# Optimization experiments

Hardware: AMD Instinct MI355X
Metric: run time of the kernel (lower is better)

Reference implementation:

```python
import jax, jax.numpy as jnp
import numpy as np
from jax import lax

B, C, H, W = 2, 96, 96, 96
N = 8            # d_state
R = C // 16      # dt_rank = 6
K = 4            # scan directions


def _gn(x, g, b, eps=1e-5):
    # GroupNorm(num_groups=1): normalize over (C,H,W) per sample, per-channel affine
    mu = jnp.mean(x, axis=(1, 2, 3), keepdims=True)
    var = jnp.var(x, axis=(1, 2, 3), keepdims=True)
    xn = (x - mu) * jax.lax.rsqrt(var + eps)
    return xn * g[None, :, None, None] + b[None, :, None, None]


def _conv1x1(x, w, b):
    return jnp.einsum('bchw,oc->bohw', x, w) + b[None, :, None, None]


def _ss2d(x, xproj_w, dt_w, dt_b, A_log, Ds):
    # x: [B,C,H,W]. 4-directional selective scan (VMamba SS2D core).
    Bn, Cc, Hh, Ww = x.shape
    L = Hh * Ww
    x_hw = x.reshape(Bn, Cc, L)                                   # row-major
    x_wh = jnp.transpose(x, (0, 1, 3, 2)).reshape(Bn, Cc, L)      # col-major
    xs = jnp.stack([x_hw, x_wh, x_hw[..., ::-1], x_wh[..., ::-1]], axis=1)  # [B,K,C,L]
    xdbl = jnp.einsum('bkcl,kdc->bkdl', xs, xproj_w)              # [B,K,R+2N,L]
    dts, Bs, Cs = jnp.split(xdbl, [R, R + N], axis=2)             # [B,K,R,L],[B,K,N,L],[B,K,N,L]
    dts = jax.nn.softplus(jnp.einsum('bkrl,kcr->bkcl', dts, dt_w) + dt_b[None, :, :, None])  # [B,K,C,L]
    A = -jnp.exp(A_log)                                           # [K,C,N]
    dA = jnp.exp(dts[:, :, :, None, :] * A[None, :, :, :, None])                    # [B,K,C,N,L]
    dBx = dts[:, :, :, None, :] * Bs[:, :, None, :, :] * xs[:, :, :, None, :]       # [B,K,C,N,L]

    def comb(e1, e2):
        a1, b1 = e1
        a2, b2 = e2
        return a1 * a2, a2 * b1 + b2

    _, hs = lax.associative_scan(comb, (dA, dBx), axis=-1)        # h_t = dA_t*h_{t-1} + dBx_t
    ys = jnp.einsum('bkcnl,bknl->bkcl', hs, Cs) + Ds[None, :, :, None] * xs
    y0 = ys[:, 0]
    y1 = jnp.transpose(ys[:, 1].reshape(Bn, Cc, Ww, Hh), (0, 1, 3, 2)).reshape(Bn, Cc, L)
    y2 = ys[:, 2][..., ::-1]
    y3 = jnp.transpose(ys[:, 3][..., ::-1].reshape(Bn, Cc, Ww, Hh), (0, 1, 3, 2)).reshape(Bn, Cc, L)
    return (y0 + y1 + y2 + y3).reshape(Bn, Cc, Hh, Ww)


def setup_inputs() -> dict:
    key = jax.random.key(0)
    ks = jax.random.split(key, 12)
    f = lambda k, sh: jax.random.normal(k, sh, jnp.float32) * 0.02
    return {
        'x': jax.random.normal(ks[0], (B, C, H, W), jnp.float32),
        'ln_g': jnp.ones((C,), jnp.float32), 'ln_b': jnp.zeros((C,), jnp.float32),
        'p1_w': f(ks[1], (C, C)), 'p1_b': jnp.zeros((C,), jnp.float32),
        'p2_w': f(ks[2], (C, C)), 'p2_b': jnp.zeros((C,), jnp.float32),
        'dw_w': f(ks[3], (C, 1, 3, 3)), 'dw_b': jnp.zeros((C,), jnp.float32),
        'xproj_w': f(ks[4], (K, R + 2 * N, C)),
        'dt_w': f(ks[5], (K, C, R)), 'dt_b': f(ks[6], (K, C)),
        'A_log': jnp.log(jnp.broadcast_to(jnp.arange(1, N + 1, dtype=jnp.float32), (K, C, N))),
        'Ds': jnp.ones((K, C), jnp.float32),
        'n2_g': jnp.ones((C,), jnp.float32), 'n2_b': jnp.zeros((C,), jnp.float32),
        'ca_w1': f(ks[7], (C // 8, C)), 'ca_b1': jnp.zeros((C // 8,), jnp.float32),
        'ca_w2': f(ks[8], (C, C // 8)), 'ca_b2': jnp.zeros((C,), jnp.float32),
    }


def reference(x, ln_g, ln_b, p1_w, p1_b, p2_w, p2_b, dw_w, dw_b,
              xproj_w, dt_w, dt_b, A_log, Ds, n2_g, n2_b,
              ca_w1, ca_b1, ca_w2, ca_b2):
    h = _gn(x, ln_g, ln_b)
    a = jax.nn.silu(_conv1x1(h, p1_w, p1_b))                       # path 1
    b = _conv1x1(h, p2_w, p2_b)                                    # path 2
    b = lax.conv_general_dilated(b, dw_w, (1, 1), ((1, 1), (1, 1)),
                                 feature_group_count=C,
                                 dimension_numbers=('NCHW', 'OIHW', 'NCHW'))
    b = b + dw_b[None, :, None, None]
    b = jax.nn.silu(b)
    b = _ss2d(b, xproj_w, dt_w, dt_b, A_log, Ds)
    b = _gn(b, n2_g, n2_b)
    y = a * b
    # channel attention (SE-style, reduction 8)
    s = jnp.mean(y, axis=(2, 3))                                   # [B,C]
    z = jax.nn.relu(s @ ca_w1.T + ca_b1)
    attn = jax.nn.sigmoid(z @ ca_w2.T + ca_b2)
    y = y * attn[:, :, None, None]
    return x + y
```

## Files before the change

kernel.cpp:

```cpp
#include <hip/hip_runtime.h>
#include <hip/hip_bf16.h>
#include <cmath>
#include <cstdint>

constexpr int B_ = 2, C_ = 96, H_ = 96, W_ = 96, L_ = H_ * W_;
constexpr int N_ = 8, R_ = 6, K_ = 4, D_ = R_ + 2 * N_;
constexpr int CH_ = 128, G_ = L_ / CH_;
constexpr int JS_ = 4, SEG_ = CH_ / JS_;
constexpr int S_ = G_ * JS_;
constexpr float EPS_ = 1e-5f;

__device__ __forceinline__ float silu_f(float v) { return v / (1.f + __expf(-v)); }
__device__ __forceinline__ float softplus_f(float t) {
    return fmaxf(t, 0.f) + __logf(1.f + __expf(-fabsf(t)));
}

__device__ __forceinline__ void block_reduce2(float& a, float& b) {
    #pragma unroll
    for (int o = 32; o; o >>= 1) { a += __shfl_xor(a, o); b += __shfl_xor(b, o); }
    __shared__ float la[4], lb[4];
    int wid = threadIdx.x >> 6;
    if ((threadIdx.x & 63) == 0) { la[wid] = a; lb[wid] = b; }
    __syncthreads();
    if (threadIdx.x == 0) { a = la[0] + la[1] + la[2] + la[3]; b = lb[0] + lb[1] + lb[2] + lb[3]; }
}

__device__ __forceinline__ void block_reduce4(float& a, float& b, float& c, float& d) {
    #pragma unroll
    for (int o = 32; o; o >>= 1) {
        a += __shfl_xor(a, o); b += __shfl_xor(b, o);
        c += __shfl_xor(c, o); d += __shfl_xor(d, o);
    }
    __shared__ float ls[4][4];
    int wid = threadIdx.x >> 6;
    if ((threadIdx.x & 63) == 0) { ls[wid][0] = a; ls[wid][1] = b; ls[wid][2] = c; ls[wid][3] = d; }
    __syncthreads();
    if (threadIdx.x == 0) {
        a = ls[0][0] + ls[1][0] + ls[2][0] + ls[3][0];
        b = ls[0][1] + ls[1][1] + ls[2][1] + ls[3][1];
        c = ls[0][2] + ls[1][2] + ls[2][2] + ls[3][2];
        d = ls[0][3] + ls[1][3] + ls[2][3] + ls[3][3];
    }
}

__global__ __launch_bounds__(256) void stats_prep_kernel(
    const float* __restrict__ in, float* __restrict__ stats,
    const float* __restrict__ lng, const float* __restrict__ lnb,
    const float* __restrict__ w1, const float* __restrict__ w2,
    float* __restrict__ wmt, float* __restrict__ pq) {
    if (blockIdx.x == 432) {
        if (blockIdx.y != 0) return;
        int t = threadIdx.x;
        if (t >= 192) return;
        int mat = t / 96, o = t % 96;
        const float* w = (mat == 0 ? w1 : w2) + o * C_;
        float* dst = wmt + ((size_t)(mat * 12 + o / 8) * C_) * 8 + (o % 8);
        float P = 0.f, Q = 0.f;
        for (int c = 0; c < C_; ++c) {
            float wv = w[c];
            float g = lng[c];
            P = fmaf(lnb[c], wv, P);
            Q = fmaf(g, wv, Q);
            dst[c * 8] = g * wv;
        }
        pq[mat * 192 + o] = P;
        pq[mat * 192 + 96 + o] = Q;
        return;
    }
    int b = blockIdx.y;
    const float* p = in + (size_t)b * ((size_t)C_ * L_);
    float s = 0.f, s2 = 0.f;
    const int total = C_ * L_;
    for (int i = blockIdx.x * 256 + threadIdx.x; i < total; i += 432 * 256) {
        float v = p[i];
        s += v;
        s2 = fmaf(v, v, s2);
    }
    block_reduce2(s, s2);
    if (threadIdx.x == 0) {
        atomicAdd(&stats[2 * b], s);
        atomicAdd(&stats[2 * b + 1], s2);
    }
}

__global__ __launch_bounds__(256) void conv1x1_kernel(
    const float* __restrict__ x, const float* __restrict__ stats,
    const float* __restrict__ wmt, const float* __restrict__ pq,
    const float* __restrict__ b1, const float* __restrict__ b2,
    float* __restrict__ a, float* __restrict__ bpre) {
    constexpr int OG = 8;
    int b = blockIdx.z, by = blockIdx.y;
    int o0 = by * OG;
    int l = blockIdx.x * 256 + threadIdx.x;

    constexpr float inv = 1.f / (float)(C_ * L_);
    float mu = stats[2 * b] * inv;
    float var = stats[2 * b + 1] * inv - mu * mu;
    float rs = rsqrtf(var + EPS_);

    const float4* w1q = (const float4*)(wmt + ((size_t)(0 * 12 + by) * C_) * 8);
    const float4* w2q = (const float4*)(wmt + ((size_t)(1 * 12 + by) * C_) * 8);

    const float* xb = x + (size_t)b * C_ * L_ + l;
    float acc1[OG], acc2[OG];
    #pragma unroll
    for (int j = 0; j < OG; ++j) { acc1[j] = 0.f; acc2[j] = 0.f; }
    #pragma unroll 4
    for (int c = 0; c < C_; ++c) {
        float xv = xb[(size_t)c * L_];
        float4 wa = w1q[2 * c];
        float4 wb = w1q[2 * c + 1];
        float4 wc = w2q[2 * c];
        float4 wd = w2q[2 * c + 1];
        acc1[0] = fmaf(xv, wa.x, acc1[0]); acc1[1] = fmaf(xv, wa.y, acc1[1]);
        acc1[2] = fmaf(xv, wa.z, acc1[2]); acc1[3] = fmaf(xv, wa.w, acc1[3]);
        acc1[4] = fmaf(xv, wb.x, acc1[4]); acc1[5] = fmaf(xv, wb.y, acc1[5]);
        acc1[6] = fmaf(xv, wb.z, acc1[6]); acc1[7] = fmaf(xv, wb.w, acc1[7]);
        acc2[0] = fmaf(xv, wc.x, acc2[0]); acc2[1] = fmaf(xv, wc.y, acc2[1]);
        acc2[2] = fmaf(xv, wc.z, acc2[2]); acc2[3] = fmaf(xv, wc.w, acc2[3]);
        acc2[4] = fmaf(xv, wd.x, acc2[4]); acc2[5] = fmaf(xv, wd.y, acc2[5]);
        acc2[6] = fmaf(xv, wd.z, acc2[6]); acc2[7] = fmaf(xv, wd.w, acc2[7]);
    }
    float murs = mu * rs;
    #pragma unroll
    for (int j = 0; j < OG; ++j) {
        int o = o0 + j;
        size_t oo = ((size_t)(b * C_ + o)) * L_ + l;
        float be1 = b1[o] + pq[o] - murs * pq[96 + o];
        float be2 = b2[o] + pq[192 + o] - murs * pq[288 + o];
        a[oo] = silu_f(fmaf(rs, acc1[j], be1));
        bpre[oo] = fmaf(rs, acc2[j], be2);
    }
}

__global__ __launch_bounds__(256) void dwt_kernel(const float* __restrict__ bp,
                                                  const float* __restrict__ wgt,
                                                  const float* __restrict__ bias,
                                                  float* __restrict__ u,
                                                  float* __restrict__ u_t) {
    int stripe = blockIdx.x, c = blockIdx.y, b = blockIdx.z;
    int h0 = stripe * 48;
    __shared__ float in_s[50][96];
    __shared__ float out_s[48][97];
    const float* in = bp + ((size_t)(b * C_ + c)) * L_;
    for (int idx = threadIdx.x; idx < 50 * 96; idx += 256) {
        int r = idx / 96, w = idx % 96;
        int hh = h0 - 1 + r;
        in_s[r][w] = (hh >= 0 && hh < 96) ? in[hh * 96 + w] : 0.f;
    }
    __syncthreads();
    const float* kw = wgt + c * 9;
    float k0 = kw[0], k1 = kw[1], k2 = kw[2], k3 = kw[3], k4 = kw[4],
          k5 = kw[5], k6 = kw[6], k7 = kw[7], k8 = kw[8];
    float bs = bias[c];
    float* up = u + ((size_t)(b * C_ + c)) * L_;
    for (int idx = threadIdx.x; idx < 48 * 96; idx += 256) {
        int r = idx / 96, w = idx % 96;
        int ri = r + 1;
        bool wl = (w > 0), wr = (w < 95);
        float acc = bs;
        acc = fmaf(wl ? in_s[ri - 1][w - 1] : 0.f, k0, acc);
        acc = fmaf(in_s[ri - 1][w], k1, acc);
        acc = fmaf(wr ? in_s[ri - 1][w + 1] : 0.f, k2, acc);
        acc = fmaf(wl ? in_s[ri][w - 1] : 0.f, k3, acc);
        acc = fmaf(in_s[ri][w], k4, acc);
        acc = fmaf(wr ? in_s[ri][w + 1] : 0.f, k5, acc);
        acc = fmaf(wl ? in_s[ri + 1][w - 1] : 0.f, k6, acc);
        acc = fmaf(in_s[ri + 1][w], k7, acc);
        acc = fmaf(wr ? in_s[ri + 1][w + 1] : 0.f, k8, acc);
        float v = silu_f(acc);
        up[(h0 + r) * 96 + w] = v;
        out_s[r][w] = v;
    }
    __syncthreads();
    float* tp = u_t + ((size_t)(b * C_ + c)) * L_;
    for (int idx = threadIdx.x; idx < 96 * 48; idx += 256) {
        int w = idx / 48, r = idx % 48;
        tp[w * 96 + h0 + r] = out_s[r][w];
    }
}

__global__ __launch_bounds__(256) void proj_kernel(
    const float* __restrict__ u, const float* __restrict__ u_t,
    const float* __restrict__ xproj,
    float* __restrict__ dts, float* __restrict__ Bsb, float* __restrict__ Csb) {
    int b = blockIdx.z, k = blockIdx.y;
    int pos = threadIdx.x & 63, cg = threadIdx.x >> 6;
    int l = blockIdx.x * 64 + pos;

    __shared__ float sxp[C_][24];
    __shared__ float red[D_][4][64];
    for (int i = threadIdx.x; i < D_ * C_; i += 256) {
        int d = i / C_, c = i % C_;
        sxp[c][d] = xproj[(k * D_ + d) * C_ + c];
    }
    __syncthreads();

    const float* src = ((k & 1) ? u_t : u) + (size_t)b * C_ * L_;
    int posIdx = (k < 2) ? l : (L_ - 1 - l);
    const float* sp = src + (size_t)(cg * 24) * L_ + posIdx;

    float acc[D_];
    #pragma unroll
    for (int d = 0; d < D_; ++d) acc[d] = 0.f;
    #pragma unroll 4
    for (int ci = 0; ci < 24; ++ci) {
        int c = cg * 24 + ci;
        float xv = sp[(size_t)ci * L_];
        float w[22];
        *(float4*)&w[0]  = *(const float4*)&sxp[c][0];
        *(float4*)&w[4]  = *(const float4*)&sxp[c][4];
        *(float4*)&w[8]  = *(const float4*)&sxp[c][8];
        *(float4*)&w[12] = *(const float4*)&sxp[c][12];
        *(float4*)&w[16] = *(const float4*)&sxp[c][16];
        *(float2*)&w[20] = *(const float2*)&sxp[c][20];
        #pragma unroll
        for (int d = 0; d < D_; ++d) acc[d] = fmaf(xv, w[d], acc[d]);
    }
    #pragma unroll
    for (int d = 0; d < D_; ++d) red[d][cg][pos] = acc[d];
    __syncthreads();

    if (cg == 0) {
        #pragma unroll
        for (int r = 0; r < R_; ++r) {
            float s = red[r][0][pos] + red[r][1][pos] + red[r][2][pos] + red[r][3][pos];
            dts[((size_t)((b * K_ + k) * R_ + r)) * L_ + l] = s;
        }
    } else if (cg == 1) {
        #pragma unroll
        for (int n = 0; n < N_; ++n) {
            int d = R_ + n;
            float s = red[d][0][pos] + red[d][1][pos] + red[d][2][pos] + red[d][3][pos];
            Bsb[((size_t)((b * K_ + k) * N_ + n)) * L_ + l] = s;
        }
    } else if (cg == 2) {
        #pragma unroll
        for (int n = 0; n < N_; ++n) {
            int d = R_ + N_ + n;
            float s = red[d][0][pos] + red[d][1][pos] + red[d][2][pos] + red[d][3][pos];
            Csb[((size_t)((b * K_ + k) * N_ + n)) * L_ + l] = s;
        }
    }
}

__global__ __launch_bounds__(192) void scan1_kernel(
    const float* __restrict__ dts, const float* __restrict__ dtw,
    const float* __restrict__ dtbv, const float* __restrict__ Bs,
    const float* __restrict__ u, const float* __restrict__ u_t,
    const float* __restrict__ A_log,
    float* __restrict__ carA, float* __restrict__ carB) {
    int g = blockIdx.x >> 1, chalf = blockIdx.x & 1;
    int k = blockIdx.y, b = blockIdx.z;
    int c0 = chalf * 48;
    const int t = threadIdx.x;
    const int l0 = g * CH_;

    __shared__ float u_s[48][133];
    __shared__ float B_s[128][12];
    __shared__ float T_s[128][8];

    const float* usrc = ((k & 1) ? u_t : u) + (size_t)b * C_ * L_ + (size_t)c0 * L_;
    if (k < 2) {
        for (int idx = t; idx < 48 * 32; idx += 192) {
            int c2 = idx >> 5, q = idx & 31;
            *(float4*)&u_s[c2][q * 4] = *(const float4*)(usrc + (size_t)c2 * L_ + l0 + q * 4);
        }
    } else {
        for (int idx = t; idx < 48 * 32; idx += 192) {
            int c2 = idx >> 5, q = idx & 31;
            float4 v = *(const float4*)(usrc + (size_t)c2 * L_ + (L_ - l0 - q * 4 - 4));
            u_s[c2][q * 4 + 0] = v.w; u_s[c2][q * 4 + 1] = v.z;
            u_s[c2][q * 4 + 2] = v.y; u_s[c2][q * 4 + 3] = v.x;
        }
    }
    const float* Bg = Bs + ((size_t)(b * K_ + k)) * N_ * L_ + l0;
    for (int idx = t; idx < 8 * 32; idx += 192) {
        int n = idx >> 5, q = idx & 31;
        float4 v = *(const float4*)(Bg + (size_t)n * L_ + q * 4);
        B_s[q * 4 + 0][n] = v.x; B_s[q * 4 + 1][n] = v.y;
        B_s[q * 4 + 2][n] = v.z; B_s[q * 4 + 3][n] = v.w;
    }
    const float* Tg = dts + ((size_t)(b * K_ + k)) * R_ * L_ + l0;
    for (int idx = t; idx < 6 * 32; idx += 192) {
        int r = idx >> 5, q = idx & 31;
        float4 v = *(const float4*)(Tg + (size_t)r * L_ + q * 4);
        T_s[q * 4 + 0][r] = v.x; T_s[q * 4 + 1][r] = v.y;
        T_s[q * 4 + 2][r] = v.z; T_s[q * 4 + 3][r] = v.w;
    }
    __syncthreads();

    int cc = t % 48, j = t / 48;
    int c = c0 + cc;
    float A[N_];
    #pragma unroll
    for (int n = 0; n < N_; ++n) A[n] = -__expf(A_log[(k * C_ + c) * N_ + n]);
    float wdt[R_];
    #pragma unroll
    for (int r = 0; r < R_; ++r) wdt[r] = dtw[(k * C_ + c) * R_ + r];
    float bdt = dtbv[k * C_ + c];

    float ap[N_], h[N_];
    #pragma unroll
    for (int n = 0; n < N_; ++n) { ap[n] = 1.f; h[n] = 0.f; }
    int i0 = j * SEG_;
    for (int ii = 0; ii < SEG_; ii += 4) {
        float4 x4 = *(float4*)&u_s[cc][i0 + ii];
        float xx[4] = {x4.x, x4.y, x4.z, x4.w};
        #pragma unroll
        for (int s = 0; s < 4; ++s) {
            int i = i0 + ii + s;
            float4 t4 = *(float4*)&T_s[i][0];
            float2 t2 = *(float2*)&T_s[i][4];
            float tt = bdt;
            tt = fmaf(t4.x, wdt[0], tt); tt = fmaf(t4.y, wdt[1], tt);
            tt = fmaf(t4.z, wdt[2], tt); tt = fmaf(t4.w, wdt[3], tt);
            tt = fmaf(t2.x, wdt[4], tt); tt = fmaf(t2.y, wdt[5], tt);
            float d = softplus_f(tt);
            float dx = d * xx[s];
            float4 ba = *(float4*)&B_s[i][0];
            float4 bb = *(float4*)&B_s[i][4];
            float bv[8] = {ba.x, ba.y, ba.z, ba.w, bb.x, bb.y, bb.z, bb.w};
            #pragma unroll
            for (int n = 0; n < N_; ++n) {
                float da = __expf(d * A[n]);
                ap[n] *= da;
                h[n] = fmaf(da, h[n], bv[n] * dx);
            }
        }
    }
    size_t sidx = (((size_t)((b * K_ + k) * C_ + c)) * S_ + (g * JS_ + j)) * N_;
    #pragma unroll
    for (int n = 0; n < N_; ++n) { carA[sidx + n] = ap[n]; carB[sidx + n] = h[n]; }
}

__global__ __launch_bounds__(256) void scan2_kernel(const float* __restrict__ carA,
                                                    const float* __restrict__ carB,
                                                    float* __restrict__ hinit) {
    int row = blockIdx.x;
    const int t = threadIdx.x;
    __shared__ float as_[S_ * N_];
    __shared__ float bs_[S_ * N_];
    const float4* Ag = (const float4*)(carA + (size_t)row * S_ * N_);
    const float4* Bg4 = (const float4*)(carB + (size_t)row * S_ * N_);
    float4* As4 = (float4*)as_;
    float4* Bs4 = (float4*)bs_;
    for (int i = t; i < S_ * N_ / 4; i += 256) { As4[i] = Ag[i]; Bs4[i] = Bg4[i]; }
    __syncthreads();

    int n = t >> 5, g = t & 31;
    int s0 = g * 9;
    float A = 1.f, Bc = 0.f;
    #pragma unroll
    for (int q = 0; q < 9; ++q) {
        int idx = (s0 + q) * N_ + n;
        float a = as_[idx], b = bs_[idx];
        Bc = fmaf(a, Bc, b);
        A = a * A;
    }
    #pragma unroll
    for (int d = 1; d < 32; d <<= 1) {
        float pA = __shfl_up(A, d, 32);
        float pB = __shfl_up(Bc, d, 32);
        if (g >= d) { Bc = fmaf(A, pB, Bc); A = A * pA; }
    }
    float h = __shfl_up(Bc, 1, 32);
    if (g == 0) h = 0.f;
    #pragma unroll
    for (int q = 0; q < 9; ++q) {
        int idx = (s0 + q) * N_ + n;
        float a = as_[idx], b = bs_[idx];
        as_[idx] = h;
        h = fmaf(a, h, b);
    }
    __syncthreads();
    float4* Hg = (float4*)(hinit + (size_t)row * S_ * N_);
    for (int i = t; i < S_ * N_ / 4; i += 256) Hg[i] = As4[i];
}

__global__ __launch_bounds__(192) void scan3_kernel(
    const float* __restrict__ dts, const float* __restrict__ dtw,
    const float* __restrict__ dtbv, const float* __restrict__ Bs,
    const float* __restrict__ Cs, const float* __restrict__ u,
    const float* __restrict__ u_t, const float* __restrict__ A_log,
    const float* __restrict__ Dsv, const float* __restrict__ hinit,
    float* __restrict__ ydir) {
    int g = blockIdx.x >> 1, chalf = blockIdx.x & 1;
    int k = blockIdx.y, b = blockIdx.z;
    int c0 = chalf * 48;
    const int t = threadIdx.x;
    const int l0 = g * CH_;

    __shared__ float u_s[48][133];
    __shared__ float B_s[128][12];
    __shared__ float C_s[128][12];
    __shared__ float T_s[128][8];

    const float* usrc = ((k & 1) ? u_t : u) + (size_t)b * C_ * L_ + (size_t)c0 * L_;
    if (k < 2) {
        for (int idx = t; idx < 48 * 32; idx += 192) {
            int c2 = idx >> 5, q = idx & 31;
            *(float4*)&u_s[c2][q * 4] = *(const float4*)(usrc + (size_t)c2 * L_ + l0 + q * 4);
        }
    } else {
        for (int idx = t; idx < 48 * 32; idx += 192) {
            int c2 = idx >> 5, q = idx & 31;
            float4 v = *(const float4*)(usrc + (size_t)c2 * L_ + (L_ - l0 - q * 4 - 4));
            u_s[c2][q * 4 + 0] = v.w; u_s[c2][q * 4 + 1] = v.z;
            u_s[c2][q * 4 + 2] = v.y; u_s[c2][q * 4 + 3] = v.x;
        }
    }
    const float* Bg = Bs + ((size_t)(b * K_ + k)) * N_ * L_ + l0;
    const float* Cg = Cs + ((size_t)(b * K_ + k)) * N_ * L_ + l0;
    for (int idx = t; idx < 8 * 32; idx += 192) {
        int n = idx >> 5, q = idx & 31;
        float4 v = *(const float4*)(Bg + (size_t)n * L_ + q * 4);
        B_s[q * 4 + 0][n] = v.x; B_s[q * 4 + 1][n] = v.y;
        B_s[q * 4 + 2][n] = v.z; B_s[q * 4 + 3][n] = v.w;
        float4 w = *(const float4*)(Cg + (size_t)n * L_ + q * 4);
        C_s[q * 4 + 0][n] = w.x; C_s[q * 4 + 1][n] = w.y;
        C_s[q * 4 + 2][n] = w.z; C_s[q * 4 + 3][n] = w.w;
    }
    const float* Tg = dts + ((size_t)(b * K_ + k)) * R_ * L_ + l0;
    for (int idx = t; idx < 6 * 32; idx += 192) {
        int r = idx >> 5, q = idx & 31;
        float4 v = *(const float4*)(Tg + (size_t)r * L_ + q * 4);
        T_s[q * 4 + 0][r] = v.x; T_s[q * 4 + 1][r] = v.y;
        T_s[q * 4 + 2][r] = v.z; T_s[q * 4 + 3][r] = v.w;
    }
    __syncthreads();

    int cc = t % 48, j = t / 48;
    int c = c0 + cc;
    float A[N_];
    #pragma unroll
    for (int n = 0; n < N_; ++n) A[n] = -__expf(A_log[(k * C_ + c) * N_ + n]);
    float wdt[R_];
    #pragma unroll
    for (int r = 0; r < R_; ++r) wdt[r] = dtw[(k * C_ + c) * R_ + r];
    float bdt = dtbv[k * C_ + c];
    float Dv = Dsv[k * C_ + c];

    float h[N_];
    size_t sidx = (((size_t)((b * K_ + k) * C_ + c)) * S_ + (g * JS_ + j)) * N_;
    #pragma unroll
    for (int n = 0; n < N_; ++n) h[n] = hinit[sidx + n];

    int i0 = j * SEG_;
    for (int ii = 0; ii < SEG_; ii += 4) {
        float4 x4 = *(float4*)&u_s[cc][i0 + ii];
        float xx[4] = {x4.x, x4.y, x4.z, x4.w};
        #pragma unroll
        for (int s = 0; s < 4; ++s) {
            int i = i0 + ii + s;
            float4 t4 = *(float4*)&T_s[i][0];
            float2 t2 = *(float2*)&T_s[i][4];
            float tt = bdt;
            tt = fmaf(t4.x, wdt[0], tt); tt = fmaf(t4.y, wdt[1], tt);
            tt = fmaf(t4.z, wdt[2], tt); tt = fmaf(t4.w, wdt[3], tt);
            tt = fmaf(t2.x, wdt[4], tt); tt = fmaf(t2.y, wdt[5], tt);
            float d = softplus_f(tt);
            float dx = d * xx[s];
            float4 ba = *(float4*)&B_s[i][0];
            float4 bb = *(float4*)&B_s[i][4];
            float4 ca = *(float4*)&C_s[i][0];
            float4 cb = *(float4*)&C_s[i][4];
            float bv[8] = {ba.x, ba.y, ba.z, ba.w, bb.x, bb.y, bb.z, bb.w};
            float cv[8] = {ca.x, ca.y, ca.z, ca.w, cb.x, cb.y, cb.z, cb.w};
            float y = Dv * xx[s];
            #pragma unroll
            for (int n = 0; n < N_; ++n) {
                float da = __expf(d * A[n]);
                h[n] = fmaf(da, h[n], bv[n] * dx);
                y = fmaf(cv[n], h[n], y);
            }
            u_s[cc][i] = y;
        }
    }
    __syncthreads();
    float* yg = ydir + ((size_t)((b * K_ + k) * C_ + c0)) * L_ + l0;
    for (int idx = t; idx < 48 * 32; idx += 192) {
        int c2 = idx >> 5, q = idx & 31;
        *(float4*)(yg + (size_t)c2 * L_ + q * 4) = *(float4*)&u_s[c2][q * 4];
    }
}

__global__ __launch_bounds__(256) void merge_kernel(const float* __restrict__ ydir,
                                                    const float* __restrict__ a,
                                                    float* __restrict__ ysum,
                                                    float* __restrict__ stats) {
    int h0 = blockIdx.x * 32;
    int c = blockIdx.y, b = blockIdx.z;
    __shared__ float t1[96][33], t3[96][33];
    const float* y0p = ydir + ((size_t)((b * K_ + 0) * C_ + c)) * L_;
    const float* y1p = ydir + ((size_t)((b * K_ + 1) * C_ + c)) * L_;
    const float* y2p = ydir + ((size_t)((b * K_ + 2) * C_ + c)) * L_;
    const float* y3p = ydir + ((size_t)((b * K_ + 3) * C_ + c)) * L_;
    for (int idx = threadIdx.x; idx < 96 * 32; idx += 256) {
        int w = idx >> 5, hh = idx & 31;
        t1[w][hh] = y1p[w * 96 + h0 + hh];
        t3[w][hh] = y3p[L_ - 1 - (w * 96 + h0 + hh)];
    }
    __syncthreads();
    float s = 0.f, s2 = 0.f, m0 = 0.f, m1 = 0.f;
    float* yout = ysum + ((size_t)(b * C_ + c)) * L_;
    const float* ap = a + ((size_t)(b * C_ + c)) * L_;
    for (int idx = threadIdx.x; idx < 32 * 96; idx += 256) {
        int hh = idx / 96, w = idx % 96;
        int pix = (h0 + hh) * 96 + w;
        float v = y0p[pix] + y2p[L_ - 1 - pix] + t1[w][hh] + t3[w][hh];
        float av = ap[pix];
        yout[pix] = v;
        s += v;
        s2 = fmaf(v, v, s2);
        m0 += av;
        m1 = fmaf(av, v, m1);
    }
    block_reduce4(s, s2, m0, m1);
    if (threadIdx.x == 0) {
        atomicAdd(&stats[4 + 2 * b], s);
        atomicAdd(&stats[5 + 2 * b], s2);
        atomicAdd(&stats[16 + b * C_ + c], m0);
        atomicAdd(&stats[256 + b * C_ + c], m1);
    }
}

__global__ __launch_bounds__(128) void attn_kernel(
    const float* __restrict__ stats, const float* __restrict__ g2,
    const float* __restrict__ b2, const float* __restrict__ w1,
    const float* __restrict__ b1, const float* __restrict__ w2,
    const float* __restrict__ b2a, float* __restrict__ attn) {
    int b = blockIdx.x;
    constexpr float inv = 1.f / (float)(C_ * L_);
    float mu = stats[4 + 2 * b] * inv;
    float var = stats[5 + 2 * b] * inv - mu * mu;
    float rs = rsqrtf(var + EPS_);
    __shared__ float ss[C_];
    __shared__ float zz[12];
    int t = threadIdx.x;
    if (t < C_) {
        float M0 = stats[16 + b * C_ + t];
        float M1 = stats[256 + b * C_ + t];
        ss[t] = (g2[t] * rs * (M1 - mu * M0) + b2[t] * M0) * (1.f / (float)L_);
    }
    __syncthreads();
    if (t < 12) {
        float acc = b1[t];
        for (int c = 0; c < C_; ++c) acc = fmaf(w1[t * C_ + c], ss[c], acc);
        zz[t] = fmaxf(acc, 0.f);
    }
    __syncthreads();
    if (t < C_) {
        float acc = b2a[t];
        #pragma unroll
        for (int j = 0; j < 12; ++j) acc = fmaf(w2[t * 12 + j], zz[j], acc);
        attn[b * C_ + t] = 1.f / (1.f + __expf(-acc));
    }
}

__global__ __launch_bounds__(256) void final_kernel(const float* __restrict__ x,
                                                    const float* __restrict__ ysum,
                                                    const float* __restrict__ a,
                                                    const float* __restrict__ stats,
                                                    const float* __restrict__ g2,
                                                    const float* __restrict__ b2,
                                                    const float* __restrict__ attn,
                                                    float* __restrict__ out) {
    int b = blockIdx.z, c = blockIdx.y;
    int pix = blockIdx.x * 256 + threadIdx.x;
    constexpr float inv = 1.f / (float)(C_ * L_);
    float mu = stats[4 + 2 * b] * inv;
    float var = stats[5 + 2 * b] * inv - mu * mu;
    float rs = rsqrtf(var + EPS_);
    float gc = g2[c] * rs, bc = b2[c] - mu * rs * g2[c];
    float at = attn[b * C_ + c];
    size_t o = ((size_t)(b * C_ + c)) * L_ + pix;
    float bn = fmaf(ysum[o], gc, bc);
    out[o] = fmaf(a[o] * bn, at, x[o]);
}

extern "C" void kernel_launch(void* const* d_in, const int* in_sizes, int n_in,
                              void* d_out, int out_size, void* d_ws, size_t ws_size,
                              hipStream_t stream) {
    const float* x    = (const float*)d_in[0];
    const float* ln_g = (const float*)d_in[1];
    const float* ln_b = (const float*)d_in[2];
    const float* p1w  = (const float*)d_in[3];
    const float* p1b  = (const float*)d_in[4];
    const float* p2w  = (const float*)d_in[5];
    const float* p2b  = (const float*)d_in[6];
    const float* dww  = (const float*)d_in[7];
    const float* dwb  = (const float*)d_in[8];
    const float* xprj = (const float*)d_in[9];
    const float* dtw  = (const float*)d_in[10];
    const float* dtb  = (const float*)d_in[11];
    const float* Alog = (const float*)d_in[12];
    const float* Dsp  = (const float*)d_in[13];
    const float* n2g  = (const float*)d_in[14];
    const float* n2b  = (const float*)d_in[15];
    const float* caw1 = (const float*)d_in[16];
    const float* cab1 = (const float*)d_in[17];
    const float* caw2 = (const float*)d_in[18];
    const float* cab2 = (const float*)d_in[19];
    float* out = (float*)d_out;

    const size_t BCL = (size_t)B_ * C_ * L_ * sizeof(float);
    char* ws = (char*)d_ws;
    size_t off = 0;
    float* stats = (float*)(ws + off); off += 4096;
    float* wmt   = (float*)(ws + off); off += 2 * 12 * 96 * 8 * sizeof(float);
    float* pq    = (float*)(ws + off); off += 2 * 2 * 96 * sizeof(float);
    float* a     = (float*)(ws + off); off += BCL;
    float* bpre  = (float*)(ws + off); off += BCL;
    float* u     = (float*)(ws + off); off += BCL;
    float* u_t   = (float*)(ws + off); off += BCL;
    float* dts   = (float*)(ws + off); off += (size_t)B_ * K_ * R_ * L_ * sizeof(float);
    float* Bsb   = (float*)(ws + off); off += (size_t)B_ * K_ * N_ * L_ * sizeof(float);
    float* Csb   = (float*)(ws + off); off += (size_t)B_ * K_ * N_ * L_ * sizeof(float);
    float* carB  = (float*)(ws + off); off += (size_t)B_ * K_ * C_ * S_ * N_ * sizeof(float);
    float* hinit = (float*)(ws + off); off += (size_t)B_ * K_ * C_ * S_ * N_ * sizeof(float);
    float* ydir  = (float*)(ws + off); off += (size_t)B_ * K_ * C_ * L_ * sizeof(float);
    float* carA = bpre;
    float* ysum = u;
    float* attnv = stats + 512;

    hipMemsetAsync(stats, 0, 4096, stream);

    stats_prep_kernel<<<dim3(433, 2), 256, 0, stream>>>(x, stats, ln_g, ln_b,
                                                        p1w, p2w, wmt, pq);
    conv1x1_kernel<<<dim3(36, 12, 2), 256, 0, stream>>>(x, stats, wmt, pq, p1b, p2b, a, bpre);
    dwt_kernel<<<dim3(2, 96, 2), 256, 0, stream>>>(bpre, dww, dwb, u, u_t);
    proj_kernel<<<dim3(144, 4, 2), 256, 0, stream>>>(u, u_t, xprj, dts, Bsb, Csb);
    scan1_kernel<<<dim3(2 * G_, K_, B_), 192, 0, stream>>>(dts, dtw, dtb, Bsb, u, u_t,
                                                           Alog, carA, carB);
    scan2_kernel<<<B_ * K_ * C_, 256, 0, stream>>>(carA, carB, hinit);
    scan3_kernel<<<dim3(2 * G_, K_, B_), 192, 0, stream>>>(dts, dtw, dtb, Bsb, Csb, u, u_t,
                                                           Alog, Dsp, hinit, ydir);
    merge_kernel<<<dim3(3, 96, 2), 256, 0, stream>>>(ydir, a, ysum, stats);
    attn_kernel<<<2, 128, 0, stream>>>(stats, n2g, n2b, caw1, cab1, caw2, cab2, attnv);
    final_kernel<<<dim3(36, 96, 2), 256, 0, stream>>>(x, ysum, a, stats, n2g, n2b, attnv, out);
}
```

Before: 269.9 us.

## Fuse all stages into one persistent cooperative kernel with grid syncs

Replaces the ten separate kernel launches with a single cooperative persistent kernel that loops over virtual blocks for each stage and separates stages with grid-wide syncs. The attention MLP is folded into the final stage and recomputed per block. The goal is to remove per-launch overhead and the gaps between launches. In exchange, the scan stages now run with 256 threads instead of 192, occupancy is capped by the largest shared-memory footprint, and grid.sync has its own cost.

```diff
diff --git a/kernel.cpp b/kernel.cpp
--- a/kernel.cpp
+++ b/kernel.cpp
@@ -1,7 +1,10 @@
 #include <hip/hip_runtime.h>
 #include <hip/hip_bf16.h>
+#include <hip/hip_cooperative_groups.h>
 #include <cmath>
 #include <cstdint>
+
+namespace cg = cooperative_groups;
 
 constexpr int B_ = 2, C_ = 96, H_ = 96, W_ = 96, L_ = H_ * W_;
 constexpr int N_ = 8, R_ = 6, K_ = 4, D_ = R_ + 2 * N_;
@@ -23,6 +26,7 @@
     if ((threadIdx.x & 63) == 0) { la[wid] = a; lb[wid] = b; }
     __syncthreads();
     if (threadIdx.x == 0) { a = la[0] + la[1] + la[2] + la[3]; b = lb[0] + lb[1] + lb[2] + lb[3]; }
+    __syncthreads();
 }
 
 __device__ __forceinline__ void block_reduce4(float& a, float& b, float& c, float& d) {
@@ -41,569 +45,506 @@
         c = ls[0][2] + ls[1][2] + ls[2][2] + ls[3][2];
         d = ls[0][3] + ls[1][3] + ls[2][3] + ls[3][3];
     }
+    __syncthreads();
 }
 
-__global__ __launch_bounds__(256) void stats_prep_kernel(
-    const float* __restrict__ in, float* __restrict__ stats,
-    const float* __restrict__ lng, const float* __restrict__ lnb,
-    const float* __restrict__ w1, const float* __restrict__ w2,
-    float* __restrict__ wmt, float* __restrict__ pq) {
-    if (blockIdx.x == 432) {
-        if (blockIdx.y != 0) return;
-        int t = threadIdx.x;
-        if (t >= 192) return;
-        int mat = t / 96, o = t % 96;
-        const float* w = (mat == 0 ? w1 : w2) + o * C_;
-        float* dst = wmt + ((size_t)(mat * 12 + o / 8) * C_) * 8 + (o % 8);
-        float P = 0.f, Q = 0.f;
+struct DwtS   { float in_s[50][96]; float out_s[48][97]; };
+struct ProjS  { float sxp[96][24]; float red[22][4][64]; };
+struct Scan1S { float u_s[48][133]; float B_s[128][12]; float T_s[128][8]; };
+struct Scan2S { float as_[S_ * N_]; float bs_[S_ * N_]; };
+struct Scan3S { float u_s[48][133]; float B_s[128][12]; float C_s[128][12]; float T_s[128][8]; };
+struct MergeS { float t1[96][33]; float t3[96][33]; };
+struct FinalS { float zz[12]; float atv; };
+
+struct P {
+    const float *x, *lng, *lnb, *p1w, *p1b, *p2w, *p2b, *dww, *dwb, *xprj,
+                *dtw, *dtb, *Alog, *Dsp, *n2g, *n2b, *caw1, *cab1, *caw2, *cab2;
+    float *stats, *wmt, *pq, *a, *bpre, *u, *u_t, *dts, *Bsb, *Csb,
+          *carA, *carB, *hinit, *ydir, *ysum, *out;
+};
+
+__global__ __launch_bounds__(256, 2) void mono_kernel(P p) {
+    cg::grid_group grid = cg::this_grid();
+    __shared__ __align__(16) char smem[41984];
+    const int t = threadIdx.x;
+    const int GS = gridDim.x;
+
+    for (int vb = blockIdx.x; vb < 865; vb += GS) {
+        if (vb < 864) {
+            int bx = vb % 432, b = vb / 432;
+            const float* ptr = p.x + (size_t)b * C_ * L_;
+            float s = 0.f, s2 = 0.f;
+            for (int i = bx * 256 + t; i < C_ * L_; i += 432 * 256) {
+                float v = ptr[i];
+                s += v;
+                s2 = fmaf(v, v, s2);
+            }
+            block_reduce2(s, s2);
+            if (t == 0) {
+                atomicAdd(&p.stats[2 * b], s);
+                atomicAdd(&p.stats[2 * b + 1], s2);
+            }
+        } else if (t < 192) {
+            int mat = t / 96, o = t % 96;
+            const float* w = (mat == 0 ? p.p1w : p.p2w) + o * C_;
+            float* dst = p.wmt + ((size_t)(mat * 12 + o / 8) * C_) * 8 + (o % 8);
+            float Pv = 0.f, Qv = 0.f;
+            for (int c = 0; c < C_; ++c) {
+                float wv = w[c];
+                float g = p.lng[c];
+                Pv = fmaf(p.lnb[c], wv, Pv);
+                Qv = fmaf(g, wv, Qv);
+                dst[c * 8] = g * wv;
+            }
+            p.pq[mat * 192 + o] = Pv;
+            p.pq[mat * 192 + 96 + o] = Qv;
+        }
+        __syncthreads();
+    }
+    grid.sync();
+
+    for (int vb = blockIdx.x; vb < 864; vb += GS) {
+        constexpr int OG = 8;
+        int lx = vb % 36, by = (vb / 36) % 12, b = vb / 432;
+        int o0 = by * OG;
+        int l = lx * 256 + t;
+        constexpr float inv = 1.f / (float)(C_ * L_);
+        float mu = p.stats[2 * b] * inv;
+        float var = p.stats[2 * b + 1] * inv - mu * mu;
+        float rs = rsqrtf(var + EPS_);
+        const float4* w1q = (const float4*)(p.wmt + ((size_t)(0 * 12 + by) * C_) * 8);
+        const float4* w2q = (const float4*)(p.wmt + ((size_t)(1 * 12 + by) * C_) * 8);
+        const float* xb = p.x + (size_t)b * C_ * L_ + l;
+        float acc1[OG], acc2[OG];
+        #pragma unroll
+        for (int j = 0; j < OG; ++j) { acc1[j] = 0.f; acc2[j] = 0.f; }
+        #pragma unroll 4
         for (int c = 0; c < C_; ++c) {
-            float wv = w[c];
-            float g = lng[c];
-            P = fmaf(lnb[c], wv, P);
-            Q = fmaf(g, wv, Q);
-            dst[c * 8] = g * wv;
-        }
-        pq[mat * 192 + o] = P;
-        pq[mat * 192 + 96 + o] = Q;
-        return;
-    }
-    int b = blockIdx.y;
-    const float* p = in + (size_t)b * ((size_t)C_ * L_);
-    float s = 0.f, s2 = 0.f;
-    const int total = C_ * L_;
-    for (int i = blockIdx.x * 256 + threadIdx.x; i < total; i += 432 * 256) {
-        float v = p[i];
-        s += v;
-        s2 = fmaf(v, v, s2);
-    }
-    block_reduce2(s, s2);
-    if (threadIdx.x == 0) {
-        atomicAdd(&stats[2 * b], s);
-        atomicAdd(&stats[2 * b + 1], s2);
-    }
-}
-
-__global__ __launch_bounds__(256) void conv1x1_kernel(
-    const float* __restrict__ x, const float* __restrict__ stats,
-    const float* __restrict__ wmt, const float* __restrict__ pq,
-    const float* __restrict__ b1, const float* __restrict__ b2,
-    float* __restrict__ a, float* __restrict__ bpre) {
-    constexpr int OG = 8;
-    int b = blockIdx.z, by = blockIdx.y;
-    int o0 = by * OG;
-    int l = blockIdx.x * 256 + threadIdx.x;
-
-    constexpr float inv = 1.f / (float)(C_ * L_);
-    float mu = stats[2 * b] * inv;
-    float var = stats[2 * b + 1] * inv - mu * mu;
-    float rs = rsqrtf(var + EPS_);
-
-    const float4* w1q = (const float4*)(wmt + ((size_t)(0 * 12 + by) * C_) * 8);
-    const float4* w2q = (const float4*)(wmt + ((size_t)(1 * 12 + by) * C_) * 8);
-
-    const float* xb = x + (size_t)b * C_ * L_ + l;
-    float acc1[OG], acc2[OG];
-    #pragma unroll
-    for (int j = 0; j < OG; ++j) { acc1[j] = 0.f; acc2[j] = 0.f; }
-    #pragma unroll 4
-    for (int c = 0; c < C_; ++c) {
-        float xv = xb[(size_t)c * L_];
-        float4 wa = w1q[2 * c];
-        float4 wb = w1q[2 * c + 1];
-        float4 wc = w2q[2 * c];
-        float4 wd = w2q[2 * c + 1];
-        acc1[0] = fmaf(xv, wa.x, acc1[0]); acc1[1] = fmaf(xv, wa.y, acc1[1]);
-        acc1[2] = fmaf(xv, wa.z, acc1[2]); acc1[3] = fmaf(xv, wa.w, acc1[3]);
-        acc1[4] = fmaf(xv, wb.x, acc1[4]); acc1[5] = fmaf(xv, wb.y, acc1[5]);
-        acc1[6] = fmaf(xv, wb.z, acc1[6]); acc1[7] = fmaf(xv, wb.w, acc1[7]);
-        acc2[0] = fmaf(xv, wc.x, acc2[0]); acc2[1] = fmaf(xv, wc.y, acc2[1]);
-        acc2[2] = fmaf(xv, wc.z, acc2[2]); acc2[3] = fmaf(xv, wc.w, acc2[3]);
-        acc2[4] = fmaf(xv, wd.x, acc2[4]); acc2[5] = fmaf(xv, wd.y, acc2[5]);
-        acc2[6] = fmaf(xv, wd.z, acc2[6]); acc2[7] = fmaf(xv, wd.w, acc2[7]);
-    }
-    float murs = mu * rs;
-    #pragma unroll
-    for (int j = 0; j < OG; ++j) {
-        int o = o0 + j;
-        size_t oo = ((size_t)(b * C_ + o)) * L_ + l;
-        float be1 = b1[o] + pq[o] - murs * pq[96 + o];
-        float be2 = b2[o] + pq[192 + o] - murs * pq[288 + o];
-        a[oo] = silu_f(fmaf(rs, acc1[j], be1));
-        bpre[oo] = fmaf(rs, acc2[j], be2);
-    }
-}
-
-__global__ __launch_bounds__(256) void dwt_kernel(const float* __restrict__ bp,
-                                                  const float* __restrict__ wgt,
-                                                  const float* __restrict__ bias,
-                                                  float* __restrict__ u,
-                                                  float* __restrict__ u_t) {
-    int stripe = blockIdx.x, c = blockIdx.y, b = blockIdx.z;
-    int h0 = stripe * 48;
-    __shared__ float in_s[50][96];
-    __shared__ float out_s[48][97];
-    const float* in = bp + ((size_t)(b * C_ + c)) * L_;
-    for (int idx = threadIdx.x; idx < 50 * 96; idx += 256) {
-        int r = idx / 96, w = idx % 96;
-        int hh = h0 - 1 + r;
-        in_s[r][w] = (hh >= 0 && hh < 96) ? in[hh * 96 + w] : 0.f;
-    }
-    __syncthreads();
-    const float* kw = wgt + c * 9;
-    float k0 = kw[0], k1 = kw[1], k2 = kw[2], k3 = kw[3], k4 = kw[4],
-          k5 = kw[5], k6 = kw[6], k7 = kw[7], k8 = kw[8];
-    float bs = bias[c];
-    float* up = u + ((size_t)(b * C_ + c)) * L_;
-    for (int idx = threadIdx.x; idx < 48 * 96; idx += 256) {
-        int r = idx / 96, w = idx % 96;
-        int ri = r + 1;
-        bool wl = (w > 0), wr = (w < 95);
-        float acc = bs;
-        acc = fmaf(wl ? in_s[ri - 1][w - 1] : 0.f, k0, acc);
-        acc = fmaf(in_s[ri - 1][w], k1, acc);
-        acc = fmaf(wr ? in_s[ri - 1][w + 1] : 0.f, k2, acc);
-        acc = fmaf(wl ? in_s[ri][w - 1] : 0.f, k3, acc);
-        acc = fmaf(in_s[ri][w], k4, acc);
-        acc = fmaf(wr ? in_s[ri][w + 1] : 0.f, k5, acc);
-        acc = fmaf(wl ? in_s[ri + 1][w - 1] : 0.f, k6, acc);
-        acc = fmaf(in_s[ri + 1][w], k7, acc);
-        acc = fmaf(wr ? in_s[ri + 1][w + 1] : 0.f, k8, acc);
-        float v = silu_f(acc);
-        up[(h0 + r) * 96 + w] = v;
-        out_s[r][w] = v;
-    }
-    __syncthreads();
-    float* tp = u_t + ((size_t)(b * C_ + c)) * L_;
-    for (int idx = threadIdx.x; idx < 96 * 48; idx += 256) {
-        int w = idx / 48, r = idx % 48;
-        tp[w * 96 + h0 + r] = out_s[r][w];
-    }
-}
-
-__global__ __launch_bounds__(256) void proj_kernel(
-    const float* __restrict__ u, const float* __restrict__ u_t,
-    const float* __restrict__ xproj,
-    float* __restrict__ dts, float* __restrict__ Bsb, float* __restrict__ Csb) {
-    int b = blockIdx.z, k = blockIdx.y;
-    int pos = threadIdx.x & 63, cg = threadIdx.x >> 6;
-    int l = blockIdx.x * 64 + pos;
-
-    __shared__ float sxp[C_][24];
-    __shared__ float red[D_][4][64];
-    for (int i = threadIdx.x; i < D_ * C_; i += 256) {
-        int d = i / C_, c = i % C_;
-        sxp[c][d] = xproj[(k * D_ + d) * C_ + c];
-    }
-    __syncthreads();
-
-    const float* src = ((k & 1) ? u_t : u) + (size_t)b * C_ * L_;
-    int posIdx = (k < 2) ? l : (L_ - 1 - l);
-    const float* sp = src + (size_t)(cg * 24) * L_ + posIdx;
-
-    float acc[D_];
-    #pragma unroll
-    for (int d = 0; d < D_; ++d) acc[d] = 0.f;
-    #pragma unroll 4
-    for (int ci = 0; ci < 24; ++ci) {
-        int c = cg * 24 + ci;
-        float xv = sp[(size_t)ci * L_];
-        float w[22];
-        *(float4*)&w[0]  = *(const float4*)&sxp[c][0];
-        *(float4*)&w[4]  = *(const float4*)&sxp[c][4];
-        *(float4*)&w[8]  = *(const float4*)&sxp[c][8];
-        *(float4*)&w[12] = *(const float4*)&sxp[c][12];
-        *(float4*)&w[16] = *(const float4*)&sxp[c][16];
-        *(float2*)&w[20] = *(const float2*)&sxp[c][20];
+            float xv = xb[(size_t)c * L_];
+            float4 wa = w1q[2 * c];
+            float4 wb = w1q[2 * c + 1];
+            float4 wc = w2q[2 * c];
+            float4 wd = w2q[2 * c + 1];
+            acc1[0] = fmaf(xv, wa.x, acc1[0]); acc1[1] = fmaf(xv, wa.y, acc1[1]);
+            acc1[2] = fmaf(xv, wa.z, acc1[2]); acc1[3] = fmaf(xv, wa.w, acc1[3]);
+            acc1[4] = fmaf(xv, wb.x, acc1[4]); acc1[5] = fmaf(xv, wb.y, acc1[5]);
+            acc1[6] = fmaf(xv, wb.z, acc1[6]); acc1[7] = fmaf(xv, wb.w, acc1[7]);
+            acc2[0] = fmaf(xv, wc.x, acc2[0]); acc2[1] = fmaf(xv, wc.y, acc2[1]);
+            acc2[2] = fmaf(xv, wc.z, acc2[2]); acc2[3] = fmaf(xv, wc.w, acc2[3]);
+            acc2[4] = fmaf(xv, wd.x, acc2[4]); acc2[5] = fmaf(xv, wd.y, acc2[5]);
+            acc2[6] = fmaf(xv, wd.z, acc2[6]); acc2[7] = fmaf(xv, wd.w, acc2[7]);
+        }
+        float murs = mu * rs;
         #pragma unroll
-        for (int d = 0; d < D_; ++d) acc[d] = fmaf(xv, w[d], acc[d]);
-    }
-    #pragma unroll
-    for (int d = 0; d < D_; ++d) red[d][cg][pos] = acc[d];
-    __syncthreads();
-
-    if (cg == 0) {
+        for (int j = 0; j < OG; ++j) {
+            int o = o0 + j;
+            size_t oo = ((size_t)(b * C_ + o)) * L_ + l;
+            float be1 = p.p1b[o] + p.pq[o] - murs * p.pq[96 + o];
+            float be2 = p.p2b[o] + p.pq[192 + o] - murs * p.pq[288 + o];
+            p.a[oo] = silu_f(fmaf(rs, acc1[j], be1));
+            p.bpre[oo] = fmaf(rs, acc2[j], be2);
+        }
+    }
+    grid.sync();
+
+    for (int vb = blockIdx.x; vb < 384; vb += GS) {
+        DwtS& S = *(DwtS*)smem;
+        int stripe = vb % 2, c = (vb / 2) % 96, b = vb / 192;
+        int h0 = stripe * 48;
+        const float* in = p.bpre + ((size_t)(b * C_ + c)) * L_;
+        for (int idx = t; idx < 50 * 96; idx += 256) {
+            int r = idx / 96, w = idx % 96;
+            int hh = h0 - 1 + r;
+            S.in_s[r][w] = (hh >= 0 && hh < 96) ? in[hh * 96 + w] : 0.f;
+        }
+        __syncthreads();
+        const float* kw = p.dww + c * 9;
+        float k0 = kw[0], k1 = kw[1], k2 = kw[2], k3 = kw[3], k4 = kw[4],
+              k5 = kw[5], k6 = kw[6], k7 = kw[7], k8 = kw[8];
+        float bs = p.dwb[c];
+        float* up = p.u + ((size_t)(b * C_ + c)) * L_;
+        for (int idx = t; idx < 48 * 96; idx += 256) {
+            int r = idx / 96, w = idx % 96;
+            int ri = r + 1;
+            bool wl = (w > 0), wr = (w < 95);
+            float acc = bs;
+            acc = fmaf(wl ? S.in_s[ri - 1][w - 1] : 0.f, k0, acc);
+            acc = fmaf(S.in_s[ri - 1][w], k1, acc);
+            acc = fmaf(wr ? S.in_s[ri - 1][w + 1] : 0.f, k2, acc);
+            acc = fmaf(wl ? S.in_s[ri][w - 1] : 0.f, k3, acc);
+            acc = fmaf(S.in_s[ri][w], k4, acc);
+            acc = fmaf(wr ? S.in_s[ri][w + 1] : 0.f, k5, acc);
+            acc = fmaf(wl ? S.in_s[ri + 1][w - 1] : 0.f, k6, acc);
+            acc = fmaf(S.in_s[ri + 1][w], k7, acc);
+            acc = fmaf(wr ? S.in_s[ri + 1][w + 1] : 0.f, k8, acc);
+            float v = silu_f(acc);
+            up[(h0 + r) * 96 + w] = v;
+            S.out_s[r][w] = v;
+        }
+        __syncthreads();
+        float* tp = p.u_t + ((size_t)(b * C_ + c)) * L_;
+        for (int idx = t; idx < 96 * 48; idx += 256) {
+            int w = idx / 48, r = idx % 48;
+            tp[w * 96 + h0 + r] = S.out_s[r][w];
+        }
+        __syncthreads();
+    }
+    grid.sync();
+
+    for (int vb = blockIdx.x; vb < 1152; vb += GS) {
+        ProjS& S = *(ProjS*)smem;
+        int lx = vb % 144, k = (vb / 144) % 4, b = vb / 576;
+        int pos = t & 63, cgp = t >> 6;
+        int l = lx * 64 + pos;
+        for (int i = t; i < D_ * C_; i += 256) {
+            int d = i / C_, c = i % C_;
+            S.sxp[c][d] = p.xprj[(k * D_ + d) * C_ + c];
+        }
+        __syncthreads();
+        const float* src = ((k & 1) ? p.u_t : p.u) + (size_t)b * C_ * L_;
+        int posIdx = (k < 2) ? l : (L_ - 1 - l);
+        const float* sp = src + (size_t)(cgp * 24) * L_ + posIdx;
+        float acc[D_];
         #pragma unroll
-        for (int r = 0; r < R_; ++r) {
-            float s = red[r][0][pos] + red[r][1][pos] + red[r][2][pos] + red[r][3][pos];
-            dts[((size_t)((b * K_ + k) * R_ + r)) * L_ + l] = s;
-        }
-    } else if (cg == 1) {
+        for (int d = 0; d < D_; ++d) acc[d] = 0.f;
+        #pragma unroll 4
+        for (int ci = 0; ci < 24; ++ci) {
+            int c = cgp * 24 + ci;
+            float xv = sp[(size_t)ci * L_];
+            float w[22];
+            *(float4*)&w[0]  = *(const float4*)&S.sxp[c][0];
+            *(float4*)&w[4]  = *(const float4*)&S.sxp[c][4];
+            *(float4*)&w[8]  = *(const float4*)&S.sxp[c][8];
+            *(float4*)&w[12] = *(const float4*)&S.sxp[c][12];
+            *(float4*)&w[16] = *(const float4*)&S.sxp[c][16];
+            *(float2*)&w[20] = *(const float2*)&S.sxp[c][20];
+            #pragma unroll
+            for (int d = 0; d < D_; ++d) acc[d] = fmaf(xv, w[d], acc[d]);
+        }
         #pragma unroll
-        for (int n = 0; n < N_; ++n) {
-            int d = R_ + n;
-            float s = red[d][0][pos] + red[d][1][pos] + red[d][2][pos] + red[d][3][pos];
-            Bsb[((size_t)((b * K_ + k) * N_ + n)) * L_ + l] = s;
-        }
-    } else if (cg == 2) {
+        for (int d = 0; d < D_; ++d) S.red[d][cgp][pos] = acc[d];
+        __syncthreads();
+        if (cgp == 0) {
+            #pragma unroll
+            for (int r = 0; r < R_; ++r) {
+                float s = S.red[r][0][pos] + S.red[r][1][pos] + S.red[r][2][pos] + S.red[r][3][pos];
+                p.dts[((size_t)((b * K_ + k) * R_ + r)) * L_ + l] = s;
+            }
+        } else if (cgp == 1) {
+            #pragma unroll
+            for (int n = 0; n < N_; ++n) {
+                int d = R_ + n;
+                float s = S.red[d][0][pos] + S.red[d][1][pos] + S.red[d][2][pos] + S.red[d][3][pos];
+                p.Bsb[((size_t)((b * K_ + k) * N_ + n)) * L_ + l] = s;
+            }
+        } else if (cgp == 2) {
+            #pragma unroll
+            for (int n = 0; n < N_; ++n) {
+                int d = R_ + N_ + n;
+                float s = S.red[d][0][pos] + S.red[d][1][pos] + S.red[d][2][pos] + S.red[d][3][pos];
+                p.Csb[((size_t)((b * K_ + k) * N_ + n)) * L_ + l] = s;
+            }
+        }
+        __syncthreads();
+    }
+    grid.sync();
+
+    for (int vb = blockIdx.x; vb < 1152; vb += GS) {
+        Scan1S& S = *(Scan1S*)smem;
+        int gx = vb % 144, k = (vb / 144) % 4, b = vb / 576;
+        int g = gx >> 1, chalf = gx & 1;
+        int c0 = chalf * 48;
+        const int l0 = g * CH_;
+        const float* usrc = ((k & 1) ? p.u_t : p.u) + (size_t)b * C_ * L_ + (size_t)c0 * L_;
+        if (k < 2) {
+            for (int idx = t; idx < 48 * 32; idx += 256) {
+                int c2 = idx >> 5, q = idx & 31;
+                *(float4*)&S.u_s[c2][q * 4] = *(const float4*)(usrc + (size_t)c2 * L_ + l0 + q * 4);
+            }
+        } else {
+            for (int idx = t; idx < 48 * 32; idx += 256) {
+                int c2 = idx >> 5, q = idx & 31;
+                float4 v = *(const float4*)(usrc + (size_t)c2 * L_ + (L_ - l0 - q * 4 - 4));
+                S.u_s[c2][q * 4 + 0] = v.w; S.u_s[c2][q * 4 + 1] = v.z;
+                S.u_s[c2][q * 4 + 2] = v.y; S.u_s[c2][q * 4 + 3] = v.x;
+            }
+        }
+        const float* Bg = p.Bsb + ((size_t)(b * K_ + k)) * N_ * L_ + l0;
+        for (int idx = t; idx < 8 * 32; idx += 256) {
+            int n = idx >> 5, q = idx & 31;
+            float4 v = *(const float4*)(Bg + (size_t)n * L_ + q * 4);
+            S.B_s[q * 4 + 0][n] = v.x; S.B_s[q * 4 + 1][n] = v.y;
+            S.B_s[q * 4 + 2][n] = v.z; S.B_s[q * 4 + 3][n] = v.w;
+        }
+        const float* Tg = p.dts + ((size_t)(b * K_ + k)) * R_ * L_ + l0;
+        for (int idx = t; idx < 6 * 32; idx += 256) {
+            int r = idx >> 5, q = idx & 31;
+            float4 v = *(const float4*)(Tg + (size_t)r * L_ + q * 4);
+            S.T_s[q * 4 + 0][r] = v.x; S.T_s[q * 4 + 1][r] = v.y;
+            S.T_s[q * 4 + 2][r] = v.z; S.T_s[q * 4 + 3][r] = v.w;
+        }
+        __syncthreads();
+        if (t < 192) {
+            int cc = t % 48, j = t / 48;
+            int c = c0 + cc;
+            float A[N_];
+            #pragma unroll
+            for (int n = 0; n < N_; ++n) A[n] = -__expf(p.Alog[(k * C_ + c) * N_ + n]);
+            float wdt[R_];
+            #pragma unroll
+            for (int r = 0; r < R_; ++r) wdt[r] = p.dtw[(k * C_ + c) * R_ + r];
+            float bdt = p.dtb[k * C_ + c];
+            float ap[N_], h[N_];
+            #pragma unroll
+            for (int n = 0; n < N_; ++n) { ap[n] = 1.f; h[n] = 0.f; }
+            int i0 = j * SEG_;
+            for (int ii = 0; ii < SEG_; ii += 4) {
+                float4 x4 = *(float4*)&S.u_s[cc][i0 + ii];
+                float xx[4] = {x4.x, x4.y, x4.z, x4.w};
+                #pragma unroll
+                for (int s = 0; s < 4; ++s) {
+                    int i = i0 + ii + s;
+                    float4 t4 = *(float4*)&S.T_s[i][0];
+                    float2 t2 = *(float2*)&S.T_s[i][4];
+                    float tt = bdt;
+                    tt = fmaf(t4.x, wdt[0], tt); tt = fmaf(t4.y, wdt[1], tt);
+                    tt = fmaf(t4.z, wdt[2], tt); tt = fmaf(t4.w, wdt[3], tt);
+                    tt = fmaf(t2.x, wdt[4], tt); tt = fmaf(t2.y, wdt[5], tt);
+                    float d = softplus_f(tt);
+                    float dx = d * xx[s];
+                    float4 ba = *(float4*)&S.B_s[i][0];
+                    float4 bb = *(float4*)&S.B_s[i][4];
+                    float bv[8] = {ba.x, ba.y, ba.z, ba.w, bb.x, bb.y, bb.z, bb.w};
+                    #pragma unroll
+                    for (int n = 0; n < N_; ++n) {
+                        float da = __expf(d * A[n]);
+                        ap[n] *= da;
+                        h[n] = fmaf(da, h[n], bv[n] * dx);
+                    }
+                }
+            }
+            size_t sidx = (((size_t)((b * K_ + k) * C_ + c)) * S_ + (g * JS_ + j)) * N_;
+            #pragma unroll
+            for (int n = 0; n < N_; ++n) { p.carA[sidx + n] = ap[n]; p.carB[sidx + n] = h[n]; }
+        }
+        __syncthreads();
+    }
+    grid.sync();
+
+    for (int vb = blockIdx.x; vb < 768; vb += GS) {
+        Scan2S& S = *(Scan2S*)smem;
+        int row = vb;
+        const float4* Ag = (const float4*)(p.carA + (size_t)row * S_ * N_);
+        const float4* Bg4 = (const float4*)(p.carB + (size_t)row * S_ * N_);
+        float4* As4 = (float4*)S.as_;
+        float4* Bs4 = (float4*)S.bs_;
+        for (int i = t; i < S_ * N_ / 4; i += 256) { As4[i] = Ag[i]; Bs4[i] = Bg4[i]; }
+        __syncthreads();
+        int n = t >> 5, g = t & 31;
+        int s0 = g * 9;
+        float A = 1.f, Bc = 0.f;
         #pragma unroll
-        for (int n = 0; n < N_; ++n) {
-            int d = R_ + N_ + n;
-            float s = red[d][0][pos] + red[d][1][pos] + red[d][2][pos] + red[d][3][pos];
-            Csb[((size_t)((b * K_ + k) * N_ + n)) * L_ + l] = s;
-        }
-    }
-}
-
-__global__ __launch_bounds__(192) void scan1_kernel(
-    const float* __restrict__ dts, const float* __restrict__ dtw,
-    const float* __restrict__ dtbv, const float* __restrict__ Bs,
-    const float* __restrict__ u, const float* __restrict__ u_t,
-    const float* __restrict__ A_log,
-    float* __restrict__ carA, float* __restrict__ carB) {
-    int g = blockIdx.x >> 1, chalf = blockIdx.x & 1;
-    int k = blockIdx.y, b = blockIdx.z;
-    int c0 = chalf * 48;
-    const int t = threadIdx.x;
-    const int l0 = g * CH_;
-
-    __shared__ float u_s[48][133];
-    __shared__ float B_s[128][12];
-    __shared__ float T_s[128][8];
-
-    const float* usrc = ((k & 1) ? u_t : u) + (size_t)b * C_ * L_ + (size_t)c0 * L_;
-    if (k < 2) {
-        for (int idx = t; idx < 48 * 32; idx += 192) {
+        for (int q = 0; q < 9; ++q) {
+            int idx = (s0 + q) * N_ + n;
+            float a = S.as_[idx], b = S.bs_[idx];
+            Bc = fmaf(a, Bc, b);
+            A = a * A;
+        }
+        #pragma unroll
+        for (int d = 1; d < 32; d <<= 1) {
+            float pA = __shfl_up(A, d, 32);
+            float pB = __shfl_up(Bc, d, 32);
+            if (g >= d) { Bc = fmaf(A, pB, Bc); A = A * pA; }
+        }
+        float h = __shfl_up(Bc, 1, 32);
+        if (g == 0) h = 0.f;
+        #pragma unroll
+        for (int q = 0; q < 9; ++q) {
+            int idx = (s0 + q) * N_ + n;
+            float a = S.as_[idx], b = S.bs_[idx];
+            S.as_[idx] = h;
+            h = fmaf(a, h, b);
+        }
+        __syncthreads();
+        float4* Hg = (float4*)(p.hinit + (size_t)row * S_ * N_);
+        for (int i = t; i < S_ * N_ / 4; i += 256) Hg[i] = As4[i];
+        __syncthreads();
+    }
+    grid.sync();
+
+    for (int vb = blockIdx.x; vb < 1152; vb += GS) {
+        Scan3S& S = *(Scan3S*)smem;
+        int gx = vb % 144, k = (vb / 144) % 4, b = vb / 576;
+        int g = gx >> 1, chalf = gx & 1;
+        int c0 = chalf * 48;
+        const int l0 = g * CH_;
+        const float* usrc = ((k & 1) ? p.u_t : p.u) + (size_t)b * C_ * L_ + (size_t)c0 * L_;
+        if (k < 2) {
+            for (int idx = t; idx < 48 * 32; idx += 256) {
+                int c2 = idx >> 5, q = idx & 31;
+                *(float4*)&S.u_s[c2][q * 4] = *(const float4*)(usrc + (size_t)c2 * L_ + l0 + q * 4);
+            }
+        } else {
+            for (int idx = t; idx < 48 * 32; idx += 256) {
+                int c2 = idx >> 5, q = idx & 31;
+                float4 v = *(const float4*)(usrc + (size_t)c2 * L_ + (L_ - l0 - q * 4 - 4));
+                S.u_s[c2][q * 4 + 0] = v.w; S.u_s[c2][q * 4 + 1] = v.z;
+                S.u_s[c2][q * 4 + 2] = v.y; S.u_s[c2][q * 4 + 3] = v.x;
+            }
+        }
+        const float* Bg = p.Bsb + ((size_t)(b * K_ + k)) * N_ * L_ + l0;
+        const float* Cg = p.Csb + ((size_t)(b * K_ + k)) * N_ * L_ + l0;
+        for (int idx = t; idx < 8 * 32; idx += 256) {
+            int n = idx >> 5, q = idx & 31;
+            float4 v = *(const float4*)(Bg + (size_t)n * L_ + q * 4);
+            S.B_s[q * 4 + 0][n] = v.x; S.B_s[q * 4 + 1][n] = v.y;
+            S.B_s[q * 4 + 2][n] = v.z; S.B_s[q * 4 + 3][n] = v.w;
+            float4 w = *(const float4*)(Cg + (size_t)n * L_ + q * 4);
+            S.C_s[q * 4 + 0][n] = w.x; S.C_s[q * 4 + 1][n] = w.y;
+            S.C_s[q * 4 + 2][n] = w.z; S.C_s[q * 4 + 3][n] = w.w;
+        }
+        const float* Tg = p.dts + ((size_t)(b * K_ + k)) * R_ * L_ + l0;
+        for (int idx = t; idx < 6 * 32; idx += 256) {
+            int r = idx >> 5, q = idx & 31;
+            float4 v = *(const float4*)(Tg + (size_t)r * L_ + q * 4);
+            S.T_s[q * 4 + 0][r] = v.x; S.T_s[q * 4 + 1][r] = v.y;
+            S.T_s[q * 4 + 2][r] = v.z; S.T_s[q * 4 + 3][r] = v.w;
+        }
+        __syncthreads();
+        if (t < 192) {
+            int cc = t % 48, j = t / 48;
+            int c = c0 + cc;
+            float A[N_];
+            #pragma unroll
+            for (int n = 0; n < N_; ++n) A[n] = -__expf(p.Alog[(k * C_ + c) * N_ + n]);
+            float wdt[R_];
+            #pragma unroll
+            for (int r = 0; r < R_; ++r) wdt[r] = p.dtw[(k * C_ + c) * R_ + r];
+            float bdt = p.dtb[k * C_ + c];
+            float Dv = p.Dsp[k * C_ + c];
+            float h[N_];
+            size_t sidx = (((size_t)((b * K_ + k) * C_ + c)) * S_ + (g * JS_ + j)) * N_;
+            #pragma unroll
+            for (int n = 0; n < N_; ++n) h[n] = p.hinit[sidx + n];
+            int i0 = j * SEG_;
+            for (int ii = 0; ii < SEG_; ii += 4) {
+                float4 x4 = *(float4*)&S.u_s[cc][i0 + ii];
+                float xx[4] = {x4.x, x4.y, x4.z, x4.w};
+                #pragma unroll
+                for (int s = 0; s < 4; ++s) {
+                    int i = i0 + ii + s;
+                    float4 t4 = *(float4*)&S.T_s[i][0];
+                    float2 t2 = *(float2*)&S.T_s[i][4];
+                    float tt = bdt;
+                    tt = fmaf(t4.x, wdt[0], tt); tt = fmaf(t4.y, wdt[1], tt);
+                    tt = fmaf(t4.z, wdt[2], tt); tt = fmaf(t4.w, wdt[3], tt);
+                    tt = fmaf(t2.x, wdt[4], tt); tt = fmaf(t2.y, wdt[5], tt);
+                    float d = softplus_f(tt);
+                    float dx = d * xx[s];
+                    float4 ba = *(float4*)&S.B_s[i][0];
+                    float4 bb = *(float4*)&S.B_s[i][4];
+                    float4 ca = *(float4*)&S.C_s[i][0];
+                    float4 cb = *(float4*)&S.C_s[i][4];
+                    float bv[8] = {ba.x, ba.y, ba.z, ba.w, bb.x, bb.y, bb.z, bb.w};
+                    float cv[8] = {ca.x, ca.y, ca.z, ca.w, cb.x, cb.y, cb.z, cb.w};
+                    float y = Dv * xx[s];
+                    #pragma unroll
+                    for (int n = 0; n < N_; ++n) {
+                        float da = __expf(d * A[n]);
+                        h[n] = fmaf(da, h[n], bv[n] * dx);
+                        y = fmaf(cv[n], h[n], y);
+                    }
+                    S.u_s[cc][i] = y;
+                }
+            }
+        }
+        __syncthreads();
+        float* yg = p.ydir + ((size_t)((b * K_ + k) * C_ + c0)) * L_ + l0;
+        for (int idx = t; idx < 48 * 32; idx += 256) {
             int c2 = idx >> 5, q = idx & 31;
-            *(float4*)&u_s[c2][q * 4] = *(const float4*)(usrc + (size_t)c2 * L_ + l0 + q * 4);
-        }
-    } else {
-        for (int idx = t; idx < 48 * 32; idx += 192) {
-            int c2 = idx >> 5, q = idx & 31;
-            float4 v = *(const float4*)(usrc + (size_t)c2 * L_ + (L_ - l0 - q * 4 - 4));
-            u_s[c2][q * 4 + 0] = v.w; u_s[c2][q * 4 + 1] = v.z;
-            u_s[c2][q * 4 + 2] = v.y; u_s[c2][q * 4 + 3] = v.x;
-        }
-    }
-    const float* Bg = Bs + ((size_t)(b * K_ + k)) * N_ * L_ + l0;
-    for (int idx = t; idx < 8 * 32; idx += 192) {
-        int n = idx >> 5, q = idx & 31;
-        float4 v = *(const float4*)(Bg + (size_t)n * L_ + q * 4);
-        B_s[q * 4 + 0][n] = v.x; B_s[q * 4 + 1][n] = v.y;
-        B_s[q * 4 + 2][n] = v.z; B_s[q * 4 + 3][n] = v.w;
-    }
-    const float* Tg = dts + ((size_t)(b * K_ + k)) * R_ * L_ + l0;
-    for (int idx = t; idx < 6 * 32; idx += 192) {
-        int r = idx >> 5, q = idx & 31;
-        float4 v = *(const float4*)(Tg + (size_t)r * L_ + q * 4);
-        T_s[q * 4 + 0][r] = v.x; T_s[q * 4 + 1][r] = v.y;
-        T_s[q * 4 + 2][r] = v.z; T_s[q * 4 + 3][r] = v.w;
-    }
-    __syncthreads();
-
-    int cc = t % 48, j = t / 48;
-    int c = c0 + cc;
-    float A[N_];
-    #pragma unroll
-    for (int n = 0; n < N_; ++n) A[n] = -__expf(A_log[(k * C_ + c) * N_ + n]);
-    float wdt[R_];
-    #pragma unroll
-    for (int r = 0; r < R_; ++r) wdt[r] = dtw[(k * C_ + c) * R_ + r];
-    float bdt = dtbv[k * C_ + c];
-
-    float ap[N_], h[N_];
-    #pragma unroll
-    for (int n = 0; n < N_; ++n) { ap[n] = 1.f; h[n] = 0.f; }
-    int i0 = j * SEG_;
-    for (int ii = 0; ii < SEG_; ii += 4) {
-        float4 x4 = *(float4*)&u_s[cc][i0 + ii];
-        float xx[4] = {x4.x, x4.y, x4.z, x4.w};
-        #pragma unroll
-        for (int s = 0; s < 4; ++s) {
-            int i = i0 + ii + s;
-            float4 t4 = *(float4*)&T_s[i][0];
-            float2 t2 = *(float2*)&T_s[i][4];
-            float tt = bdt;
-            tt = fmaf(t4.x, wdt[0], tt); tt = fmaf(t4.y, wdt[1], tt);
-            tt = fmaf(t4.z, wdt[2], tt); tt = fmaf(t4.w, wdt[3], tt);
-            tt = fmaf(t2.x, wdt[4], tt); tt = fmaf(t2.y, wdt[5], tt);
-            float d = softplus_f(tt);
-            float dx = d * xx[s];
-            float4 ba = *(float4*)&B_s[i][0];
-            float4 bb = *(float4*)&B_s[i][4];
-            float bv[8] = {ba.x, ba.y, ba.z, ba.w, bb.x, bb.y, bb.z, bb.w};
-            #pragma unroll
-            for (int n = 0; n < N_; ++n) {
-                float da = __expf(d * A[n]);
-                ap[n] *= da;
-                h[n] = fmaf(da, h[n], bv[n] * dx);
-            }
-        }
-    }
-    size_t sidx = (((size_t)((b * K_ + k) * C_ + c)) * S_ + (g * JS_ + j)) * N_;
-    #pragma unroll
-    for (int n = 0; n < N_; ++n) { carA[sidx + n] = ap[n]; carB[sidx + n] = h[n]; }
-}
-
-__global__ __launch_bounds__(256) void scan2_kernel(const float* __restrict__ carA,
-                                                    const float* __restrict__ carB,
-                                                    float* __restrict__ hinit) {
-    int row = blockIdx.x;
-    const int t = threadIdx.x;
-    __shared__ float as_[S_ * N_];
-    __shared__ float bs_[S_ * N_];
-    const float4* Ag = (const float4*)(carA + (size_t)row * S_ * N_);
-    const float4* Bg4 = (const float4*)(carB + (size_t)row * S_ * N_);
-    float4* As4 = (float4*)as_;
-    float4* Bs4 = (float4*)bs_;
-    for (int i = t; i < S_ * N_ / 4; i += 256) { As4[i] = Ag[i]; Bs4[i] = Bg4[i]; }
-    __syncthreads();
-
-    int n = t >> 5, g = t & 31;
-    int s0 = g * 9;
-    float A = 1.f, Bc = 0.f;
-    #pragma unroll
-    for (int q = 0; q < 9; ++q) {
-        int idx = (s0 + q) * N_ + n;
-        float a = as_[idx], b = bs_[idx];
-        Bc = fmaf(a, Bc, b);
-        A = a * A;
-    }
-    #pragma unroll
-    for (int d = 1; d < 32; d <<= 1) {
-        float pA = __shfl_up(A, d, 32);
-        float pB = __shfl_up(Bc, d, 32);
-        if (g >= d) { Bc = fmaf(A, pB, Bc); A = A * pA; }
-    }
-    float h = __shfl_up(Bc, 1, 32);
-    if (g == 0) h = 0.f;
-    #pragma unroll
-    for (int q = 0; q < 9; ++q) {
-        int idx = (s0 + q) * N_ + n;
-        float a = as_[idx], b = bs_[idx];
-        as_[idx] = h;
-        h = fmaf(a, h, b);
-    }
-    __syncthreads();
-    float4* Hg = (float4*)(hinit + (size_t)row * S_ * N_);
-    for (int i = t; i < S_ * N_ / 4; i += 256) Hg[i] = As4[i];
-}
-
-__global__ __launch_bounds__(192) void scan3_kernel(
-    const float* __restrict__ dts, const float* __restrict__ dtw,
-    const float* __restrict__ dtbv, const float* __restrict__ Bs,
-    const float* __restrict__ Cs, const float* __restrict__ u,
-    const float* __restrict__ u_t, const float* __restrict__ A_log,
-    const float* __restrict__ Dsv, const float* __restrict__ hinit,
-    float* __restrict__ ydir) {
-    int g = blockIdx.x >> 1, chalf = blockIdx.x & 1;
-    int k = blockIdx.y, b = blockIdx.z;
-    int c0 = chalf * 48;
-    const int t = threadIdx.x;
-    const int l0 = g * CH_;
-
-    __shared__ float u_s[48][133];
-    __shared__ float B_s[128][12];
-    __shared__ float C_s[128][12];
-    __shared__ float T_s[128][8];
-
-    const float* usrc = ((k & 1) ? u_t : u) + (size_t)b * C_ * L_ + (size_t)c0 * L_;
-    if (k < 2) {
-        for (int idx = t; idx < 48 * 32; idx += 192) {
-            int c2 = idx >> 5, q = idx & 31;
-            *(float4*)&u_s[c2][q * 4] = *(const float4*)(usrc + (size_t)c2 * L_ + l0 + q * 4);
-        }
-    } else {
-        for (int idx = t; idx < 48 * 32; idx += 192) {
-            int c2 = idx >> 5, q = idx & 31;
-            float4 v = *(const float4*)(usrc + (size_t)c2 * L_ + (L_ - l0 - q * 4 - 4));
-            u_s[c2][q * 4 + 0] = v.w; u_s[c2][q * 4 + 1] = v.z;
-            u_s[c2][q * 4 + 2] = v.y; u_s[c2][q * 4 + 3] = v.x;
-        }
-    }
-    const float* Bg = Bs + ((size_t)(b * K_ + k)) * N_ * L_ + l0;
-    const float* Cg = Cs + ((size_t)(b * K_ + k)) * N_ * L_ + l0;
-    for (int idx = t; idx < 8 * 32; idx += 192) {
-        int n = idx >> 5, q = idx & 31;
-        float4 v = *(const float4*)(Bg + (size_t)n * L_ + q * 4);
-        B_s[q * 4 + 0][n] = v.x; B_s[q * 4 + 1][n] = v.y;
-        B_s[q * 4 + 2][n] = v.z; B_s[q * 4 + 3][n] = v.w;
-        float4 w = *(const float4*)(Cg + (size_t)n * L_ + q * 4);
-        C_s[q * 4 + 0][n] = w.x; C_s[q * 4 + 1][n] = w.y;
-        C_s[q * 4 + 2][n] = w.z; C_s[q * 4 + 3][n] = w.w;
-    }
-    const float* Tg = dts + ((size_t)(b * K_ + k)) * R_ * L_ + l0;
-    for (int idx = t; idx < 6 * 32; idx += 192) {
-        int r = idx >> 5, q = idx & 31;
-        float4 v = *(const float4*)(Tg + (size_t)r * L_ + q * 4);
-        T_s[q * 4 + 0][r] = v.x; T_s[q * 4 + 1][r] = v.y;
-        T_s[q * 4 + 2][r] = v.z; T_s[q * 4 + 3][r] = v.w;
-    }
-    __syncthreads();
-
-    int cc = t % 48, j = t / 48;
-    int c = c0 + cc;
-    float A[N_];
-    #pragma unroll
-    for (int n = 0; n < N_; ++n) A[n] = -__expf(A_log[(k * C_ + c) * N_ + n]);
-    float wdt[R_];
-    #pragma unroll
-    for (int r = 0; r < R_; ++r) wdt[r] = dtw[(k * C_ + c) * R_ + r];
-    float bdt = dtbv[k * C_ + c];
-    float Dv = Dsv[k * C_ + c];
-
-    float h[N_];
-    size_t sidx = (((size_t)((b * K_ + k) * C_ + c)) * S_ + (g * JS_ + j)) * N_;
-    #pragma unroll
-    for (int n = 0; n < N_; ++n) h[n] = hinit[sidx + n];
-
-    int i0 = j * SEG_;
-    for (int ii = 0; ii < SEG_; ii += 4) {
-        float4 x4 = *(float4*)&u_s[cc][i0 + ii];
-        float xx[4] = {x4.x, x4.y, x4.z, x4.w};
-        #pragma unroll
-        for (int s = 0; s < 4; ++s) {
-            int i = i0 + ii + s;
-            float4 t4 = *(float4*)&T_s[i][0];
-            float2 t2 = *(float2*)&T_s[i][4];
-            float tt = bdt;
-            tt = fmaf(t4.x, wdt[0], tt); tt = fmaf(t4.y, wdt[1], tt);
-            tt = fmaf(t4.z, wdt[2], tt); tt = fmaf(t4.w, wdt[3], tt);
-            tt = fmaf(t2.x, wdt[4], tt); tt = fmaf(t2.y, wdt[5], tt);
-            float d = softplus_f(tt);
-            float dx = d * xx[s];
-            float4 ba = *(float4*)&B_s[i][0];
-            float4 bb = *(float4*)&B_s[i][4];
-            float4 ca = *(float4*)&C_s[i][0];
-            float4 cb = *(float4*)&C_s[i][4];
-            float bv[8] = {ba.x, ba.y, ba.z, ba.w, bb.x, bb.y, bb.z, bb.w};
-            float cv[8] = {ca.x, ca.y, ca.z, ca.w, cb.x, cb.y, cb.z, cb.w};
-            float y = Dv * xx[s];
-            #pragma unroll
-            for (int n = 0; n < N_; ++n) {
-                float da = __expf(d * A[n]);
-                h[n] = fmaf(da, h[n], bv[n] * dx);
-                y = fmaf(cv[n], h[n], y);
-            }
-            u_s[cc][i] = y;
-        }
-    }
-    __syncthreads();
-    float* yg = ydir + ((size_t)((b * K_ + k) * C_ + c0)) * L_ + l0;
-    for (int idx = t; idx < 48 * 32; idx += 192) {
-        int c2 = idx >> 5, q = idx & 31;
-        *(float4*)(yg + (size_t)c2 * L_ + q * 4) = *(float4*)&u_s[c2][q * 4];
-    }
-}
-
-__global__ __launch_bounds__(256) void merge_kernel(const float* __restrict__ ydir,
-                                                    const float* __restrict__ a,
-                                                    float* __restrict__ ysum,
-                                                    float* __restrict__ stats) {
-    int h0 = blockIdx.x * 32;
-    int c = blockIdx.y, b = blockIdx.z;
-    __shared__ float t1[96][33], t3[96][33];
-    const float* y0p = ydir + ((size_t)((b * K_ + 0) * C_ + c)) * L_;
-    const float* y1p = ydir + ((size_t)((b * K_ + 1) * C_ + c)) * L_;
-    const float* y2p = ydir + ((size_t)((b * K_ + 2) * C_ + c)) * L_;
-    const float* y3p = ydir + ((size_t)((b * K_ + 3) * C_ + c)) * L_;
-    for (int idx = threadIdx.x; idx < 96 * 32; idx += 256) {
-        int w = idx >> 5, hh = idx & 31;
-        t1[w][hh] = y1p[w * 96 + h0 + hh];
-        t3[w][hh] = y3p[L_ - 1 - (w * 96 + h0 + hh)];
-    }
-    __syncthreads();
-    float s = 0.f, s2 = 0.f, m0 = 0.f, m1 = 0.f;
-    float* yout = ysum + ((size_t)(b * C_ + c)) * L_;
-    const float* ap = a + ((size_t)(b * C_ + c)) * L_;
-    for (int idx = threadIdx.x; idx < 32 * 96; idx += 256) {
-        int hh = idx / 96, w = idx % 96;
-        int pix = (h0 + hh) * 96 + w;
-        float v = y0p[pix] + y2p[L_ - 1 - pix] + t1[w][hh] + t3[w][hh];
-        float av = ap[pix];
-        yout[pix] = v;
-        s += v;
-        s2 = fmaf(v, v, s2);
-        m0 += av;
-        m1 = fmaf(av, v, m1);
-    }
-    block_reduce4(s, s2, m0, m1);
-    if (threadIdx.x == 0) {
-        atomicAdd(&stats[4 + 2 * b], s);
-        atomicAdd(&stats[5 + 2 * b], s2);
-        atomicAdd(&stats[16 + b * C_ + c], m0);
-        atomicAdd(&stats[256 + b * C_ + c], m1);
-    }
-}
-
-__global__ __launch_bounds__(128) void attn_kernel(
-    const float* __restrict__ stats, const float* __restrict__ g2,
-    const float* __restrict__ b2, const float* __restrict__ w1,
-    const float* __restrict__ b1, const float* __restrict__ w2,
-    const float* __restrict__ b2a, float* __restrict__ attn) {
-    int b = blockIdx.x;
-    constexpr float inv = 1.f / (float)(C_ * L_);
-    float mu = stats[4 + 2 * b] * inv;
-    float var = stats[5 + 2 * b] * inv - mu * mu;
-    float rs = rsqrtf(var + EPS_);
-    __shared__ float ss[C_];
-    __shared__ float zz[12];
-    int t = threadIdx.x;
-    if (t < C_) {
-        float M0 = stats[16 + b * C_ + t];
-        float M1 = stats[256 + b * C_ + t];
-        ss[t] = (g2[t] * rs * (M1 - mu * M0) + b2[t] * M0) * (1.f / (float)L_);
-    }
-    __syncthreads();
-    if (t < 12) {
-        float acc = b1[t];
-        for (int c = 0; c < C_; ++c) acc = fmaf(w1[t * C_ + c], ss[c], acc);
-        zz[t] = fmaxf(acc, 0.f);
-    }
-    __syncthreads();
-    if (t < C_) {
-        float acc = b2a[t];
-        #pragma unroll
-        for (int j = 0; j < 12; ++j) acc = fmaf(w2[t * 12 + j], zz[j], acc);
-        attn[b * C_ + t] = 1.f / (1.f + __expf(-acc));
-    }
-}
-
-__global__ __launch_bounds__(256) void final_kernel(const float* __restrict__ x,
-                                                    const float* __restrict__ ysum,
-                                                    const float* __restrict__ a,
-                                                    const float* __restrict__ stats,
-                                                    const float* __restrict__ g2,
-                                                    const float* __restrict__ b2,
-                                                    const float* __restrict__ attn,
-                                                    float* __restrict__ out) {
-    int b = blockIdx.z, c = blockIdx.y;
-    int pix = blockIdx.x * 256 + threadIdx.x;
-    constexpr float inv = 1.f / (float)(C_ * L_);
-    float mu = stats[4 + 2 * b] * inv;
-    float var = stats[5 + 2 * b] * inv - mu * mu;
-    float rs = rsqrtf(var + EPS_);
-    float gc = g2[c] * rs, bc = b2[c] - mu * rs * g2[c];
-    float at = attn[b * C_ + c];
-    size_t o = ((size_t)(b * C_ + c)) * L_ + pix;
-    float bn = fmaf(ysum[o], gc, bc);
-    out[o] = fmaf(a[o] * bn, at, x[o]);
+            *(float4*)(yg + (size_t)c2 * L_ + q * 4) = *(float4*)&S.u_s[c2][q * 4];
+        }
+        __syncthreads();
+    }
+    grid.sync();
+
+    for (int vb = blockIdx.x; vb < 576; vb += GS) {
+        MergeS& S = *(MergeS*)smem;
+        int hx = vb % 3, c = (vb / 3) % 96, b = vb / 288;
+        int h0 = hx * 32;
+        const float* y0p = p.ydir + ((size_t)((b * K_ + 0) * C_ + c)) * L_;
+        const float* y1p = p.ydir + ((size_t)((b * K_ + 1) * C_ + c)) * L_;
+        const float* y2p = p.ydir + ((size_t)((b * K_ + 2) * C_ + c)) * L_;
+        const float* y3p = p.ydir + ((size_t)((b * K_ + 3) * C_ + c)) * L_;
+        for (int idx = t; idx < 96 * 32; idx += 256) {
+            int w = idx >> 5, hh = idx & 31;
+            S.t1[w][hh] = y1p[w * 96 + h0 + hh];
+            S.t3[w][hh] = y3p[L_ - 1 - (w * 96 + h0 + hh)];
+        }
+        __syncthreads();
+        float s = 0.f, s2 = 0.f, m0 = 0.f, m1 = 0.f;
+        float* yout = p.ysum + ((size_t)(b * C_ + c)) * L_;
+        const float* ap = p.a + ((size_t)(b * C_ + c)) * L_;
+        for (int idx = t; idx < 32 * 96; idx += 256) {
+            int hh = idx / 96, w = idx % 96;
+            int pix = (h0 + hh) * 96 + w;
+            float v = y0p[pix] + y2p[L_ - 1 - pix] + S.t1[w][hh] + S.t3[w][hh];
+            float av = ap[pix];
+            yout[pix] = v;
+            s += v;
+            s2 = fmaf(v, v, s2);
+            m0 += av;
+            m1 = fmaf(av, v, m1);
+        }
+        block_reduce4(s, s2, m0, m1);
+        if (t == 0) {
+            atomicAdd(&p.stats[4 + 2 * b], s);
+            atomicAdd(&p.stats[5 + 2 * b], s2);
+            atomicAdd(&p.stats[16 + b * C_ + c], m0);
+            atomicAdd(&p.stats[256 + b * C_ + c], m1);
+        }
+        __syncthreads();
+    }
+    grid.sync();
+
+    for (int vb = blockIdx.x; vb < 6912; vb += GS) {
+        FinalS& S = *(FinalS*)smem;
+        int lx = vb % 36, c = (vb / 36) % 96, b = vb / 3456;
+        int pix = lx * 256 + t;
+        constexpr float inv = 1.f / (float)(C_ * L_);
+        float mu = p.stats[4 + 2 * b] * inv;
+        float var = p.stats[5 + 2 * b] * inv - mu * mu;
+        float rs = rsqrtf(var + EPS_);
+        if (t < 12) {
+            float acc = p.cab1[t];
+            for (int cc = 0; cc < C_; ++cc) {
+                float M0 = p.stats[16 + b * C_ + cc];
+                float M1 = p.stats[256 + b * C_ + cc];
+                float ss = (p.n2g[cc] * rs * (M1 - mu * M0) + p.n2b[cc] * M0) * (1.f / (float)L_);
+                acc = fmaf(p.caw1[t * C_ + cc], ss, acc);
+            }
+            S.zz[t] = fmaxf(acc, 0.f);
+        }
+        __syncthreads();
+        if (t == 0) {
+            float acc = p.cab2[c];
+            #pragma unroll
+            for (int j = 0; j < 12; ++j) acc = fmaf(p.caw2[c * 12 + j], S.zz[j], acc);
+            S.atv = 1.f / (1.f + __expf(-acc));
+        }
+        __syncthreads();
+        float at = S.atv;
+        float gc = p.n2g[c] * rs, bc = p.n2b[c] - mu * rs * p.n2g[c];
+        size_t o = ((size_t)(b * C_ + c)) * L_ + pix;
+        float bn = fmaf(p.ysum[o], gc, bc);
+        p.out[o] = fmaf(p.a[o] * bn, at, p.x[o]);
+        __syncthreads();
+    }
 }
 
 extern "C" void kernel_launch(void* const* d_in, const int* in_sizes, int n_in,
                               void* d_out, int out_size, void* d_ws, size_t ws_size,
                               hipStream_t stream) {
-    const float* x    = (const float*)d_in[0];
-    const float* ln_g = (const float*)d_in[1];
-    const float* ln_b = (const float*)d_in[2];
-    const float* p1w  = (const float*)d_in[3];
-    const float* p1b  = (const float*)d_in[4];
-    const float* p2w  = (const float*)d_in[5];
-    const float* p2b  = (const float*)d_in[6];
-    const float* dww  = (const float*)d_in[7];
-    const float* dwb  = (const float*)d_in[8];
-    const float* xprj = (const float*)d_in[9];
-    const float* dtw  = (const float*)d_in[10];
-    const float* dtb  = (const float*)d_in[11];
-    const float* Alog = (const float*)d_in[12];
-    const float* Dsp  = (const float*)d_in[13];
-    const float* n2g  = (const float*)d_in[14];
-    const float* n2b  = (const float*)d_in[15];
-    const float* caw1 = (const float*)d_in[16];
-    const float* cab1 = (const float*)d_in[17];
-    const float* caw2 = (const float*)d_in[18];
-    const float* cab2 = (const float*)d_in[19];
-    float* out = (float*)d_out;
-
     const size_t BCL = (size_t)B_ * C_ * L_ * sizeof(float);
     char* ws = (char*)d_ws;
     size_t off = 0;
@@ -620,23 +561,49 @@
     float* carB  = (float*)(ws + off); off += (size_t)B_ * K_ * C_ * S_ * N_ * sizeof(float);
     float* hinit = (float*)(ws + off); off += (size_t)B_ * K_ * C_ * S_ * N_ * sizeof(float);
     float* ydir  = (float*)(ws + off); off += (size_t)B_ * K_ * C_ * L_ * sizeof(float);
-    float* carA = bpre;
-    float* ysum = u;
-    float* attnv = stats + 512;
+
+    P prm;
+    prm.x    = (const float*)d_in[0];
+    prm.lng  = (const float*)d_in[1];
+    prm.lnb  = (const float*)d_in[2];
+    prm.p1w  = (const float*)d_in[3];
+    prm.p1b  = (const float*)d_in[4];
+    prm.p2w  = (const float*)d_in[5];
+    prm.p2b  = (const float*)d_in[6];
+    prm.dww  = (const float*)d_in[7];
+    prm.dwb  = (const float*)d_in[8];
+    prm.xprj = (const float*)d_in[9];
+    prm.dtw  = (const float*)d_in[10];
+    prm.dtb  = (const float*)d_in[11];
+    prm.Alog = (const float*)d_in[12];
+    prm.Dsp  = (const float*)d_in[13];
+    prm.n2g  = (const float*)d_in[14];
+    prm.n2b  = (const float*)d_in[15];
+    prm.caw1 = (const float*)d_in[16];
+    prm.cab1 = (const float*)d_in[17];
+    prm.caw2 = (const float*)d_in[18];
+    prm.cab2 = (const float*)d_in[19];
+    prm.stats = stats; prm.wmt = wmt; prm.pq = pq;
+    prm.a = a; prm.bpre = bpre; prm.u = u; prm.u_t = u_t;
+    prm.dts = dts; prm.Bsb = Bsb; prm.Csb = Csb;
+    prm.carA = bpre;
+    prm.carB = carB; prm.hinit = hinit; prm.ydir = ydir;
+    prm.ysum = u;
+    prm.out = (float*)d_out;
+
+    int dev = 0;
+    hipGetDevice(&dev);
+    int cus = 256;
+    hipDeviceGetAttribute(&cus, hipDeviceAttributeMultiprocessorCount, dev);
+    int nb = 0;
+    hipOccupancyMaxActiveBlocksPerMultiprocessor(&nb, mono_kernel, 256, 0);
+    if (nb < 1) nb = 1;
+    long long grid_ll = (long long)nb * (long long)cus;
+    int grid = (grid_ll > 1024) ? 1024 : (int)grid_ll;
+    if (grid < 64) grid = 64;
 
     hipMemsetAsync(stats, 0, 4096, stream);
-
-    stats_prep_kernel<<<dim3(433, 2), 256, 0, stream>>>(x, stats, ln_g, ln_b,
-                                                        p1w, p2w, wmt, pq);
-    conv1x1_kernel<<<dim3(36, 12, 2), 256, 0, stream>>>(x, stats, wmt, pq, p1b, p2b, a, bpre);
-    dwt_kernel<<<dim3(2, 96, 2), 256, 0, stream>>>(bpre, dww, dwb, u, u_t);
-    proj_kernel<<<dim3(144, 4, 2), 256, 0, stream>>>(u, u_t, xprj, dts, Bsb, Csb);
-    scan1_kernel<<<dim3(2 * G_, K_, B_), 192, 0, stream>>>(dts, dtw, dtb, Bsb, u, u_t,
-                                                           Alog, carA, carB);
-    scan2_kernel<<<B_ * K_ * C_, 256, 0, stream>>>(carA, carB, hinit);
-    scan3_kernel<<<dim3(2 * G_, K_, B_), 192, 0, stream>>>(dts, dtw, dtb, Bsb, Csb, u, u_t,
-                                                           Alog, Dsp, hinit, ydir);
-    merge_kernel<<<dim3(3, 96, 2), 256, 0, stream>>>(ydir, a, ysum, stats);
-    attn_kernel<<<2, 128, 0, stream>>>(stats, n2g, n2b, caw1, cab1, caw2, cab2, attnv);
-    final_kernel<<<dim3(36, 96, 2), 256, 0, stream>>>(x, ysum, a, stats, n2g, n2b, attnv, out);
+    void* args[] = { &prm };
+    hipLaunchCooperativeKernel((const void*)mono_kernel, dim3(grid), dim3(256),
+                               args, 0, stream);
 }
```

Result: slower. 723.9 us (+168.2%).
